# Optimization experiments

Measured on AMD Instinct MI355X. Metric: run time of the kernel, lower is better.

Reference implementation:

```python
import jax, jax.numpy as jnp
import numpy as np

NUM_HEADS = 8


def _forward(x, Wq, bq, Wk, bk, Wv, bv, Wo, bo, w1, b1, w2, b2, tau):
    B, S, E = x.shape
    H = NUM_HEADS
    hd = E // H
    scale = hd ** -0.5

    def heads(t):
        return t.reshape(B, S, H, hd).transpose(0, 2, 1, 3)  # [B,H,S,hd]

    q = heads(x @ Wq + bq)
    k = heads(x @ Wk + bk)
    v = heads(x @ Wv + bv)
    s = jnp.einsum('bhqd,bhkd->bhqk', q, k) * scale  # [B,H,S,S]

    # ---- autopoietic transform (vectorized over batch, no mask) ----
    s = jnp.clip(jnp.nan_to_num(s, nan=0.0, posinf=10.0, neginf=-10.0), -15.0, 15.0)
    ma = s.mean(axis=1)  # mean over heads -> [B,S,S]
    eps_safe = 0.05  # clamp(eps=1e-6, 0.05, 0.8)
    sa = jnp.clip(jnp.clip(ma, -8.0, 8.0) * eps_safe, -10.0, 10.0)
    # 1x1 conv on [1,1,S,S] == per-channel scalar scale+bias -> [B,C,S,S]
    hid = jax.nn.relu(jnp.clip(sa[:, None] * w1[None, :, None, None]
                               + b1[None, :, None, None], -5.0, 5.0))
    ap = jnp.clip(jnp.einsum('bcij,c->bij', hid, w2) + b2, -5.0, 5.0)
    taylor = jnp.clip(1.0 + 0.05 * (ap * 50.0), 0.5, 1.5)
    sig = jax.nn.sigmoid(taylor)
    p = jax.nn.softmax(jnp.clip(ma, -10.0, 10.0), axis=-1)
    Hent = -p * jnp.log(p + 1e-6)
    Fm = jax.nn.softmax(3.0 * Hent, axis=-1)
    t = sig * Fm
    eo = jnp.sqrt((ma * ma).sum(axis=(1, 2), keepdims=True)) + 1e-4  # fro norm
    et = jnp.sqrt((t * t).sum(axis=(1, 2), keepdims=True)) + 1e-4
    t = jnp.clip(eo / et, 0.8, 1.2) * t
    tm = t.mean(axis=(1, 2), keepdims=True)
    om = ma.mean(axis=(1, 2), keepdims=True)
    tstd = jnp.sqrt(jnp.clip(((t - tm) ** 2).mean(axis=(1, 2), keepdims=True), 0.01, None))
    ostd = jnp.sqrt(jnp.clip(((ma - om) ** 2).mean(axis=(1, 2), keepdims=True), 0.01, None))
    gd = jnp.clip(ostd / tstd, 0.8, 1.2)
    ar = jnp.clip(jnp.abs(ma).max(axis=(1, 2), keepdims=True), 1.0, 10.0)
    sm = jnp.clip(0.3 / jnp.log1p(ar), 0.1, 0.5)
    st = tm + sm * gd * (t - tm)  # scaled_transform
    ent = Hent.mean(axis=(1, 2), keepdims=True)
    ne = ent / jnp.log(jnp.float32(S))  # normalized entropy (max_entropy = log S)
    rr = 0.4 * (1.0 - jnp.clip(ne, 0.0, 0.4))  # residual ratio (base 0.4, entropy-damped)
    # blend transform back into per-head scores (res_scale = 1.0)
    s = s + rr[:, None] * (st - ma)[:, None]

    attn = jax.nn.softmax(s / tau, axis=-1)
    out = jnp.einsum('bhqk,bhkd->bhqd', attn, v)
    out = out.transpose(0, 2, 1, 3).reshape(B, S, E)
    return out @ Wo + bo


def setup_inputs() -> dict:
    key = jax.random.key(0)
    ks = jax.random.split(key, 8)
    B, S, E, C = 4, 512, 512, 128
    w_scale = 0.02
    return {
        'x': jax.random.normal(ks[0], (B, S, E), dtype=jnp.float32),
        'Wq': jax.random.normal(ks[1], (E, E), dtype=jnp.float32) * w_scale,
        'bq': jnp.zeros((E,), jnp.float32),
        'Wk': jax.random.normal(ks[2], (E, E), dtype=jnp.float32) * w_scale,
        'bk': jnp.zeros((E,), jnp.float32),
        'Wv': jax.random.normal(ks[3], (E, E), dtype=jnp.float32) * w_scale,
        'bv': jnp.zeros((E,), jnp.float32),
        'Wo': jax.random.normal(ks[4], (E, E), dtype=jnp.float32) * w_scale,
        'bo': jnp.zeros((E,), jnp.float32),
        'w1': jax.random.normal(ks[5], (C,), dtype=jnp.float32) * 0.5,
        'b1': jnp.zeros((C,), jnp.float32),
        'w2': jax.random.normal(ks[6], (C,), dtype=jnp.float32) * 0.1,
        'b2': jnp.zeros((1,), jnp.float32),
        'tau': jnp.ones((1,), jnp.float32),
    }


def reference(x, Wq, bq, Wk, bk, Wv, bv, Wo, bo, w1, b1, w2, b2, tau):
    return _forward(x, Wq, bq, Wk, bk, Wv, bv, Wo, bo, w1, b1, w2, b2, tau)
```

## Files before the change

kernel.cpp:

```cpp
#include <hip/hip_runtime.h>
#include <math.h>

#define BB 4
#define SS 512
#define EE 512
#define NH 8
#define HD 64
#define NC 128
#define NTAB 4096

typedef _Float16 f16x8 __attribute__((ext_vector_type(8)));
typedef float f32x4 __attribute__((ext_vector_type(4)));

struct HL { _Float16 h, l; };

__device__ __forceinline__ float clampf(float v, float lo, float hi) {
  return fminf(fmaxf(v, lo), hi);
}
__device__ __forceinline__ HL split16(float x) {
  HL r;
  r.h = (_Float16)x;
  r.l = (_Float16)(x - (float)r.h);
  return r;
}

__device__ __forceinline__ float waveRedSum(float v) {
#pragma unroll
  for (int o = 32; o; o >>= 1) v += __shfl_xor(v, o);
  return v;
}
__device__ __forceinline__ float waveRedMax(float v) {
#pragma unroll
  for (int o = 32; o; o >>= 1) v = fmaxf(v, __shfl_xor(v, o));
  return v;
}
__device__ __forceinline__ float blockRedSum(float v, float* red) {
  int tid = threadIdx.x;
  v = waveRedSum(v);
  __syncthreads();
  if ((tid & 63) == 0) red[tid >> 6] = v;
  __syncthreads();
  return red[0] + red[1] + red[2] + red[3];
}
__device__ __forceinline__ float blockRedMax(float v, float* red) {
  int tid = threadIdx.x;
  v = waveRedMax(v);
  __syncthreads();
  if ((tid & 63) == 0) red[tid >> 6] = v;
  __syncthreads();
  return fmaxf(fmaxf(red[0], red[1]), fmaxf(red[2], red[3]));
}

__global__ __launch_bounds__(256) void k_prep(
    const float* __restrict__ Wq, const float* __restrict__ Wk,
    const float* __restrict__ Wv, const float* __restrict__ Wo,
    _Float16* __restrict__ Wth, _Float16* __restrict__ Wtl) {
  const int j = blockIdx.x;
  const int tid = threadIdx.x;
  const int z = j >> 6;
  const int rem = j & 63;
  const int k0 = (rem & 7) * 64, n0 = (rem >> 3) * 64;
  const float* W = (z == 0) ? Wq : (z == 1) ? Wk : (z == 2) ? Wv : Wo;
  __shared__ float Tt[64][68];
  const int r = tid >> 2, c = (tid & 3) * 16;
#pragma unroll
  for (int jj = 0; jj < 16; jj += 4)
    *(float4*)&Tt[r][c + jj] =
        *(const float4*)(W + (size_t)(k0 + r) * EE + n0 + c + jj);
  __syncthreads();
  f16x8 h0, l0, h1, l1;
#pragma unroll
  for (int jj = 0; jj < 8; ++jj) {
    HL r0 = split16(Tt[c + jj][r]);
    HL r1 = split16(Tt[c + 8 + jj][r]);
    h0[jj] = r0.h; l0[jj] = r0.l;
    h1[jj] = r1.h; l1[jj] = r1.l;
  }
  _Float16* dh = Wth + ((size_t)z * EE + n0 + r) * EE + k0 + c;
  _Float16* dl = Wtl + ((size_t)z * EE + n0 + r) * EE + k0 + c;
  *(f16x8*)dh = h0;
  *(f16x8*)(dh + 8) = h1;
  *(f16x8*)dl = l0;
  *(f16x8*)(dl + 8) = l1;
}

__global__ __launch_bounds__(256) void k_qkv_mfma(
    const float* __restrict__ x,
    const _Float16* __restrict__ Wth, const _Float16* __restrict__ Wtl,
    const float* __restrict__ bq, const float* __restrict__ bk,
    const float* __restrict__ bv, const float* __restrict__ w1,
    const float* __restrict__ b1, const float* __restrict__ w2,
    const float* __restrict__ b2, float* __restrict__ T,
    _Float16* __restrict__ qh, _Float16* __restrict__ ql,
    _Float16* __restrict__ kh, _Float16* __restrict__ kl,
    _Float16* __restrict__ vth, _Float16* __restrict__ vtl) {
  const int which = blockIdx.z;
  const int tid = threadIdx.x;
  const int wave = tid >> 6, lane = tid & 63;
  const int quad = lane >> 4, l16 = lane & 15;
  const int m0 = blockIdx.y * 64;
  const int n0 = blockIdx.x * 64;
  const _Float16* Bh = Wth + (size_t)which * EE * EE;
  const _Float16* Bl = Wtl + (size_t)which * EE * EE;

  __shared__ __align__(16) char smpool[36864];
  _Float16(*LAh)[72] = (_Float16(*)[72])(smpool);
  _Float16(*LAl)[72] = (_Float16(*)[72])(smpool + 9216);
  _Float16(*LBh)[72] = (_Float16(*)[72])(smpool + 18432);
  _Float16(*LBl)[72] = (_Float16(*)[72])(smpool + 27648);
  float(*TR)[68] = (float(*)[68])(smpool);

  const int sr0 = tid >> 3, sc0 = (tid & 7) * 8;
  const int sr1 = sr0 + 32;

  float4 rx0a = *(const float4*)(x + (size_t)(m0 + sr0) * EE + sc0);
  float4 rx0b = *(const float4*)(x + (size_t)(m0 + sr0) * EE + sc0 + 4);
  float4 rx1a = *(const float4*)(x + (size_t)(m0 + sr1) * EE + sc0);
  float4 rx1b = *(const float4*)(x + (size_t)(m0 + sr1) * EE + sc0 + 4);
  f16x8 rB0h = *(const f16x8*)(Bh + (size_t)(n0 + sr0) * EE + sc0);
  f16x8 rB0l = *(const f16x8*)(Bl + (size_t)(n0 + sr0) * EE + sc0);
  f16x8 rB1h = *(const f16x8*)(Bh + (size_t)(n0 + sr1) * EE + sc0);
  f16x8 rB1l = *(const f16x8*)(Bl + (size_t)(n0 + sr1) * EE + sc0);

  f32x4 acc[4] = {};
  for (int k0 = 0; k0 < EE; k0 += 64) {
    if (k0) __syncthreads();
    {
      float f0[8] = {rx0a.x, rx0a.y, rx0a.z, rx0a.w,
                     rx0b.x, rx0b.y, rx0b.z, rx0b.w};
      float f1[8] = {rx1a.x, rx1a.y, rx1a.z, rx1a.w,
                     rx1b.x, rx1b.y, rx1b.z, rx1b.w};
      f16x8 h0, l0, h1, l1;
#pragma unroll
      for (int j = 0; j < 8; ++j) {
        HL r0 = split16(f0[j]);
        HL r1 = split16(f1[j]);
        h0[j] = r0.h; l0[j] = r0.l;
        h1[j] = r1.h; l1[j] = r1.l;
      }
      *(f16x8*)&LAh[sr0][sc0] = h0;
      *(f16x8*)&LAl[sr0][sc0] = l0;
      *(f16x8*)&LAh[sr1][sc0] = h1;
      *(f16x8*)&LAl[sr1][sc0] = l1;
    }
    *(f16x8*)&LBh[sr0][sc0] = rB0h;
    *(f16x8*)&LBl[sr0][sc0] = rB0l;
    *(f16x8*)&LBh[sr1][sc0] = rB1h;
    *(f16x8*)&LBl[sr1][sc0] = rB1l;
    __syncthreads();
    if (k0 + 64 < EE) {
      const int kn = k0 + 64;
      rx0a = *(const float4*)(x + (size_t)(m0 + sr0) * EE + kn + sc0);
      rx0b = *(const float4*)(x + (size_t)(m0 + sr0) * EE + kn + sc0 + 4);
      rx1a = *(const float4*)(x + (size_t)(m0 + sr1) * EE + kn + sc0);
      rx1b = *(const float4*)(x + (size_t)(m0 + sr1) * EE + kn + sc0 + 4);
      rB0h = *(const f16x8*)(Bh + (size_t)(n0 + sr0) * EE + kn + sc0);
      rB0l = *(const f16x8*)(Bl + (size_t)(n0 + sr0) * EE + kn + sc0);
      rB1h = *(const f16x8*)(Bh + (size_t)(n0 + sr1) * EE + kn + sc0);
      rB1l = *(const f16x8*)(Bl + (size_t)(n0 + sr1) * EE + kn + sc0);
    }
#pragma unroll
    for (int kk = 0; kk < 64; kk += 32) {
      f16x8 ah = *(const f16x8*)&LAh[wave * 16 + l16][kk + quad * 8];
      f16x8 al = *(const f16x8*)&LAl[wave * 16 + l16][kk + quad * 8];
#pragma unroll
      for (int nt = 0; nt < 4; ++nt) {
        f16x8 bhf = *(const f16x8*)&LBh[nt * 16 + l16][kk + quad * 8];
        f16x8 blf = *(const f16x8*)&LBl[nt * 16 + l16][kk + quad * 8];
        acc[nt] = __builtin_amdgcn_mfma_f32_16x16x32_f16(ah, bhf, acc[nt], 0, 0, 0);
        acc[nt] = __builtin_amdgcn_mfma_f32_16x16x32_f16(ah, blf, acc[nt], 0, 0, 0);
        acc[nt] = __builtin_amdgcn_mfma_f32_16x16x32_f16(al, bhf, acc[nt], 0, 0, 0);
      }
    }
  }
  const float* bias = (which == 0) ? bq : (which == 1) ? bk : bv;
  if (which == 2) {
    __syncthreads();
#pragma unroll
    for (int nt = 0; nt < 4; ++nt) {
      const int dcol = nt * 16 + l16;
      const float bb = bias[n0 + nt * 16 + l16];
#pragma unroll
      for (int r = 0; r < 4; ++r)
        TR[dcol][wave * 16 + quad * 4 + r] = acc[nt][r] + bb;
    }
    __syncthreads();
    const int d = tid >> 2, cc = (tid & 3) * 16;
    const int bh = (m0 >> 9) * NH + (n0 >> 6);
    const int si0 = m0 & 511;
    f16x8 h0, l0, h1, l1;
#pragma unroll
    for (int jj = 0; jj < 8; ++jj) {
      HL r0 = split16(TR[d][cc + jj]);
      HL r1 = split16(TR[d][cc + 8 + jj]);
      h0[jj] = r0.h; l0[jj] = r0.l;
      h1[jj] = r1.h; l1[jj] = r1.l;
    }
    _Float16* dh = vth + ((size_t)bh * HD + d) * SS + si0 + cc;
    _Float16* dl = vtl + ((size_t)bh * HD + d) * SS + si0 + cc;
    *(f16x8*)dh = h0;
    *(f16x8*)(dh + 8) = h1;
    *(f16x8*)dl = l0;
    *(f16x8*)(dl + 8) = l1;
  } else {
    const float postscale = (which == 0) ? 0.125f : 1.0f;
    const int mbase = m0 + wave * 16 + quad * 4;
#pragma unroll
    for (int nt = 0; nt < 4; ++nt) {
      const int col = n0 + nt * 16 + l16;
      const float bb = bias[col];
      const int hh = col >> 6, d = col & 63;
#pragma unroll
      for (int r = 0; r < 4; ++r) {
        const int mm = mbase + r;
        const int b_ = mm >> 9, si = mm & 511;
        const size_t idx = (((size_t)(b_ * NH + hh)) * SS + si) * HD + d;
        const float val = (acc[nt][r] + bb) * postscale;
        HL sp = split16(val);
        (which ? kh : qh)[idx] = sp.h;
        (which ? kl : ql)[idx] = sp.l;
      }
    }
    if (which == 0 && blockIdx.x == 0 && blockIdx.y < 17) {
      int idx = blockIdx.y * 256 + tid;
      if (idx <= NTAB) {
        float sa = -0.4f + (float)idx * (0.8f / (float)NTAB);
        float ap = 0.f;
#pragma unroll 4
        for (int c = 0; c < NC; ++c) {
          float h = fminf(fmaxf(sa * w1[c] + b1[c], 0.f), 5.f);
          ap += h * w2[c];
        }
        ap = clampf(ap + b2[0], -5.f, 5.f);
        float tay = clampf(1.0f + 0.05f * (ap * 50.0f), 0.5f, 1.5f);
        T[idx] = 1.0f / (1.0f + expf(-tay));
      }
    }
  }
}

__global__ __launch_bounds__(256) void k_scores_mfma(
    const _Float16* __restrict__ qh, const _Float16* __restrict__ ql,
    const _Float16* __restrict__ kh, const _Float16* __restrict__ kl,
    float* __restrict__ s) {
  const int bh = blockIdx.z;
  const int i0 = blockIdx.y * 64, j0 = blockIdx.x * 64;
  const int tid = threadIdx.x;
  const int wave = tid >> 6, lane = tid & 63;
  const int quad = lane >> 4, l16 = lane & 15;

  __shared__ _Float16 Qh[64][72], Ql[64][72], Kh[64][72], Kl[64][72];
  const int r = tid >> 2, c = (tid & 3) * 16;
  {
    const size_t qoff = ((size_t)bh * SS + i0 + r) * HD + c;
    const size_t koff = ((size_t)bh * SS + j0 + r) * HD + c;
    *(f16x8*)&Qh[r][c] = *(const f16x8*)(qh + qoff);
    *(f16x8*)&Qh[r][c + 8] = *(const f16x8*)(qh + qoff + 8);
    *(f16x8*)&Ql[r][c] = *(const f16x8*)(ql + qoff);
    *(f16x8*)&Ql[r][c + 8] = *(const f16x8*)(ql + qoff + 8);
    *(f16x8*)&Kh[r][c] = *(const f16x8*)(kh + koff);
    *(f16x8*)&Kh[r][c + 8] = *(const f16x8*)(kh + koff + 8);
    *(f16x8*)&Kl[r][c] = *(const f16x8*)(kl + koff);
    *(f16x8*)&Kl[r][c + 8] = *(const f16x8*)(kl + koff + 8);
  }
  __syncthreads();

  f16x8 a_hi[2], a_lo[2];
#pragma unroll
  for (int ks = 0; ks < 2; ++ks) {
    a_hi[ks] = *(const f16x8*)&Qh[wave * 16 + l16][ks * 32 + quad * 8];
    a_lo[ks] = *(const f16x8*)&Ql[wave * 16 + l16][ks * 32 + quad * 8];
  }
  f32x4 acc[4] = {};
#pragma unroll
  for (int ks = 0; ks < 2; ++ks) {
#pragma unroll
    for (int t = 0; t < 4; ++t) {
      f16x8 b_hi = *(const f16x8*)&Kh[t * 16 + l16][ks * 32 + quad * 8];
      f16x8 b_lo = *(const f16x8*)&Kl[t * 16 + l16][ks * 32 + quad * 8];
      acc[t] = __builtin_amdgcn_mfma_f32_16x16x32_f16(a_hi[ks], b_hi,
                                                      acc[t], 0, 0, 0);
      acc[t] = __builtin_amdgcn_mfma_f32_16x16x32_f16(a_hi[ks], b_lo,
                                                      acc[t], 0, 0, 0);
      acc[t] = __builtin_amdgcn_mfma_f32_16x16x32_f16(a_lo[ks], b_hi,
                                                      acc[t], 0, 0, 0);
    }
  }
  float* sb = s + (size_t)bh * SS * SS;
#pragma unroll
  for (int t = 0; t < 4; ++t) {
#pragma unroll
    for (int r2 = 0; r2 < 4; ++r2) {
      float val = clampf(acc[t][r2], -15.0f, 15.0f);
      sb[(size_t)(i0 + wave * 16 + quad * 4 + r2) * SS + j0 + t * 16 + l16] = val;
    }
  }
}

__global__ __launch_bounds__(64) void k_rowstat(
    const float* __restrict__ s, const float* __restrict__ T,
    float* __restrict__ ma, float* __restrict__ t_un,
    float* __restrict__ rowred) {
  const int row = blockIdx.x;
  const int b_ = row >> 9, i = row & 511;
  const int lane = threadIdx.x;

  float4 a0 = {0.f, 0.f, 0.f, 0.f}, a1 = {0.f, 0.f, 0.f, 0.f};
#pragma unroll
  for (int hh = 0; hh < NH; ++hh) {
    const float4* p = reinterpret_cast<const float4*>(
                          s + (((size_t)(b_ * NH + hh) * SS) + i) * SS) +
                      lane * 2;
    float4 u0 = p[0], u1 = p[1];
    a0.x += u0.x; a0.y += u0.y; a0.z += u0.z; a0.w += u0.w;
    a1.x += u1.x; a1.y += u1.y; a1.z += u1.z; a1.w += u1.w;
  }
  float m[8] = {a0.x * 0.125f, a0.y * 0.125f, a0.z * 0.125f, a0.w * 0.125f,
                a1.x * 0.125f, a1.y * 0.125f, a1.z * 0.125f, a1.w * 0.125f};
  {
    float4* mp = reinterpret_cast<float4*>(ma + ((size_t)b_ * SS + i) * SS) +
                 lane * 2;
    float4 w0 = {m[0], m[1], m[2], m[3]}, w1v = {m[4], m[5], m[6], m[7]};
    mp[0] = w0;
    mp[1] = w1v;
  }
  float sma = 0.f, sma2 = 0.f, mabs = 0.f;
#pragma unroll
  for (int e = 0; e < 8; ++e) {
    sma += m[e];
    sma2 += m[e] * m[e];
    mabs = fmaxf(mabs, fabsf(m[e]));
  }
  sma = waveRedSum(sma);
  sma2 = waveRedSum(sma2);
  mabs = waveRedMax(mabs);

  float ex[8], esum = 0.f;
#pragma unroll
  for (int e = 0; e < 8; ++e) {
    ex[e] = expf(clampf(m[e], -10.f, 10.f));
    esum += ex[e];
  }
  esum = waveRedSum(esum);
  float inv = 1.0f / esum;
  float Hv[8], sH = 0.f;
#pragma unroll
  for (int e = 0; e < 8; ++e) {
    float p = ex[e] * inv;
    Hv[e] = -p * logf(p + 1e-6f);
    sH += Hv[e];
  }
  sH = waveRedSum(sH);

  float fx[8], fsum = 0.f;
#pragma unroll
  for (int e = 0; e < 8; ++e) {
    fx[e] = expf(3.0f * Hv[e]);
    fsum += fx[e];
  }
  fsum = waveRedSum(fsum);
  float finv = 1.0f / fsum;

  float t[8], st = 0.f, st2 = 0.f;
#pragma unroll
  for (int e = 0; e < 8; ++e) {
    float sa = clampf(m[e], -8.f, 8.f) * 0.05f;
    float pos = (sa + 0.4f) * ((float)NTAB / 0.8f);
    int idx = (int)pos;
    idx = idx < 0 ? 0 : (idx > NTAB - 1 ? NTAB - 1 : idx);
    float frac = pos - (float)idx;
    float g0 = T[idx], g1 = T[idx + 1];
    float sig = g0 + (g1 - g0) * frac;
    t[e] = sig * fx[e] * finv;
    st += t[e];
    st2 += t[e] * t[e];
  }
  st = waveRedSum(st);
  st2 = waveRedSum(st2);
  {
    float4* tp = reinterpret_cast<float4*>(t_un + ((size_t)b_ * SS + i) * SS) +
                 lane * 2;
    float4 w0 = {t[0], t[1], t[2], t[3]}, w1v = {t[4], t[5], t[6], t[7]};
    tp[0] = w0;
    tp[1] = w1v;
  }
  if (lane == 0) {
    float* rp = rowred + (size_t)row * 8;
    rp[0] = sma; rp[1] = sma2; rp[2] = mabs;
    rp[3] = st;  rp[4] = st2;  rp[5] = sH;
  }
}

__global__ __launch_bounds__(256) void k_av_fused(
    const float* __restrict__ s, const float* __restrict__ ma,
    const float* __restrict__ t_un, const float* __restrict__ rowred,
    const float* __restrict__ tau, const _Float16* __restrict__ vth,
    const _Float16* __restrict__ vtl, _Float16* __restrict__ oh,
    _Float16* __restrict__ ol) {
  const int bh = blockIdx.y;
  const int b_ = bh >> 3, hh = bh & 7;
  const int m0 = blockIdx.x * 32;
  const int tid = threadIdx.x;
  const int wave = tid >> 6, lane = tid & 63;
  const int quad = lane >> 4, l16 = lane & 15;

  __shared__ float red[4];
  float c0, c1, c2;
  {
    const float* r0 = rowred + ((size_t)b_ * SS + tid * 2) * 8;
    const float* r1 = r0 + 8;
    float sma = blockRedSum(r0[0] + r1[0], red);
    float sma2 = blockRedSum(r0[1] + r1[1], red);
    float mabs = blockRedMax(fmaxf(r0[2], r1[2]), red);
    float st = blockRedSum(r0[3] + r1[3], red);
    float st2 = blockRedSum(r0[4] + r1[4], red);
    float sH = blockRedSum(r0[5] + r1[5], red);
    const float N = (float)(SS * SS);
    float eo = sqrtf(sma2) + 1e-4f;
    float et = sqrtf(st2) + 1e-4f;
    float r = clampf(eo / et, 0.8f, 1.2f);
    float tmean = r * st / N;
    float om = sma / N;
    float vart = r * r * fmaxf(st2 / N - (st / N) * (st / N), 0.f);
    float tstd = sqrtf(fmaxf(vart, 0.01f));
    float varo = fmaxf(sma2 / N - om * om, 0.f);
    float ostd = sqrtf(fmaxf(varo, 0.01f));
    float gd = clampf(ostd / tstd, 0.8f, 1.2f);
    float ar = clampf(mabs, 1.f, 10.f);
    float sm = clampf(0.3f / log1pf(ar), 0.1f, 0.5f);
    float ent = sH / N;
    float ne = ent / logf((float)SS);
    float rr = 0.4f * (1.f - clampf(ne, 0.f, 0.4f));
    float G = sm * gd;
    c0 = rr * (1.f - G) * tmean;
    c1 = rr * G * r;
    c2 = rr;
  }
  const float itau = 1.0f / tau[0];

  __shared__ _Float16 Ph[32][40], Pl[32][40];
  __shared__ float Zp[32][4];

  const bool stager = (tid < 128);
  const int srow = tid >> 2;
  const int ci = tid & 3;
  const int schunk = ci * 8;
  const size_t sbase = ((size_t)bh * SS + m0 + (srow & 31)) * SS + schunk;
  const size_t mbase = ((size_t)b_ * SS + m0 + (srow & 31)) * SS + schunk;

  float4 sv0, sv1, mv0, mv1, tv0, tv1;
  if (stager) {
    sv0 = *(const float4*)(s + sbase);
    sv1 = *(const float4*)(s + sbase + 4);
    mv0 = *(const float4*)(ma + mbase);
    mv1 = *(const float4*)(ma + mbase + 4);
    tv0 = *(const float4*)(t_un + mbase);
    tv1 = *(const float4*)(t_un + mbase + 4);
  }

  float zpart = 0.f;
  f32x4 acc[2] = {};
  for (int k0 = 0; k0 < SS; k0 += 32) {
    if (k0) __syncthreads();
    if (stager) {
      float svv[8] = {sv0.x, sv0.y, sv0.z, sv0.w, sv1.x, sv1.y, sv1.z, sv1.w};
      float mvv[8] = {mv0.x, mv0.y, mv0.z, mv0.w, mv1.x, mv1.y, mv1.z, mv1.w};
      float tvv[8] = {tv0.x, tv0.y, tv0.z, tv0.w, tv1.x, tv1.y, tv1.z, tv1.w};
      f16x8 hv, lv;
#pragma unroll
      for (int j = 0; j < 8; ++j) {
        float vv = (svv[j] + c0 + c1 * tvv[j] - c2 * mvv[j]) * itau;
        float e = expf(vv) * 1.52587890625e-05f;
        zpart += e;
        HL r = split16(e);
        hv[j] = r.h;
        lv[j] = r.l;
      }
      *(f16x8*)&Ph[srow][schunk] = hv;
      *(f16x8*)&Pl[srow][schunk] = lv;
    }
    __syncthreads();
    if (stager && k0 + 32 < SS) {
      sv0 = *(const float4*)(s + sbase + k0 + 32);
      sv1 = *(const float4*)(s + sbase + k0 + 36);
      mv0 = *(const float4*)(ma + mbase + k0 + 32);
      mv1 = *(const float4*)(ma + mbase + k0 + 36);
      tv0 = *(const float4*)(t_un + mbase + k0 + 32);
      tv1 = *(const float4*)(t_un + mbase + k0 + 36);
    }
    const size_t boff = ((size_t)bh * HD + wave * 16 + l16) * SS + k0 + quad * 8;
    f16x8 bh_ = *(const f16x8*)(vth + boff);
    f16x8 bl_ = *(const f16x8*)(vtl + boff);
#pragma unroll
    for (int mt = 0; mt < 2; ++mt) {
      f16x8 ah = *(const f16x8*)&Ph[mt * 16 + l16][quad * 8];
      f16x8 al = *(const f16x8*)&Pl[mt * 16 + l16][quad * 8];
      acc[mt] = __builtin_amdgcn_mfma_f32_16x16x32_f16(ah, bh_, acc[mt], 0, 0, 0);
      acc[mt] = __builtin_amdgcn_mfma_f32_16x16x32_f16(ah, bl_, acc[mt], 0, 0, 0);
      acc[mt] = __builtin_amdgcn_mfma_f32_16x16x32_f16(al, bh_, acc[mt], 0, 0, 0);
    }
  }
  __syncthreads();
  if (stager) Zp[srow][ci] = zpart;
  __syncthreads();
#pragma unroll
  for (int mt = 0; mt < 2; ++mt) {
#pragma unroll
    for (int r = 0; r < 4; ++r) {
      const int lr = mt * 16 + quad * 4 + r;
      const float Z = Zp[lr][0] + Zp[lr][1] + Zp[lr][2] + Zp[lr][3];
      const float oV = acc[mt][r] / Z;
      const int si = m0 + lr;
      const size_t idx =
          ((size_t)(b_ * SS + si)) * EE + hh * HD + wave * 16 + l16;
      HL sp = split16(oV);
      oh[idx] = sp.h;
      ol[idx] = sp.l;
    }
  }
}

__global__ __launch_bounds__(256) void k_out_mfma(
    const _Float16* __restrict__ oh, const _Float16* __restrict__ ol,
    const _Float16* __restrict__ Wth, const _Float16* __restrict__ Wtl,
    const float* __restrict__ bo, float* __restrict__ out) {
  const int tid = threadIdx.x;
  const int wave = tid >> 6, lane = tid & 63;
  const int quad = lane >> 4, l16 = lane & 15;
  const int m0 = blockIdx.y * 64;
  const int n0 = blockIdx.x * 64;
  const _Float16* Bh = Wth + (size_t)3 * EE * EE;
  const _Float16* Bl = Wtl + (size_t)3 * EE * EE;

  __shared__ _Float16 LAh[64][72], LAl[64][72], LBh[64][72], LBl[64][72];

  const int sr0 = tid >> 3, sc0 = (tid & 7) * 8;
  const int sr1 = sr0 + 32;

  f16x8 rA0h = *(const f16x8*)(oh + (size_t)(m0 + sr0) * EE + sc0);
  f16x8 rA0l = *(const f16x8*)(ol + (size_t)(m0 + sr0) * EE + sc0);
  f16x8 rB0h = *(const f16x8*)(Bh + (size_t)(n0 + sr0) * EE + sc0);
  f16x8 rB0l = *(const f16x8*)(Bl + (size_t)(n0 + sr0) * EE + sc0);
  f16x8 rA1h = *(const f16x8*)(oh + (size_t)(m0 + sr1) * EE + sc0);
  f16x8 rA1l = *(const f16x8*)(ol + (size_t)(m0 + sr1) * EE + sc0);
  f16x8 rB1h = *(const f16x8*)(Bh + (size_t)(n0 + sr1) * EE + sc0);
  f16x8 rB1l = *(const f16x8*)(Bl + (size_t)(n0 + sr1) * EE + sc0);

  f32x4 acc[4] = {};
  for (int k0 = 0; k0 < EE; k0 += 64) {
    if (k0) __syncthreads();
    *(f16x8*)&LAh[sr0][sc0] = rA0h;
    *(f16x8*)&LAl[sr0][sc0] = rA0l;
    *(f16x8*)&LBh[sr0][sc0] = rB0h;
    *(f16x8*)&LBl[sr0][sc0] = rB0l;
    *(f16x8*)&LAh[sr1][sc0] = rA1h;
    *(f16x8*)&LAl[sr1][sc0] = rA1l;
    *(f16x8*)&LBh[sr1][sc0] = rB1h;
    *(f16x8*)&LBl[sr1][sc0] = rB1l;
    __syncthreads();
    if (k0 + 64 < EE) {
      const int kn = k0 + 64;
      rA0h = *(const f16x8*)(oh + (size_t)(m0 + sr0) * EE + kn + sc0);
      rA0l = *(const f16x8*)(ol + (size_t)(m0 + sr0) * EE + kn + sc0);
      rB0h = *(const f16x8*)(Bh + (size_t)(n0 + sr0) * EE + kn + sc0);
      rB0l = *(const f16x8*)(Bl + (size_t)(n0 + sr0) * EE + kn + sc0);
      rA1h = *(const f16x8*)(oh + (size_t)(m0 + sr1) * EE + kn + sc0);
      rA1l = *(const f16x8*)(ol + (size_t)(m0 + sr1) * EE + kn + sc0);
      rB1h = *(const f16x8*)(Bh + (size_t)(n0 + sr1) * EE + kn + sc0);
      rB1l = *(const f16x8*)(Bl + (size_t)(n0 + sr1) * EE + kn + sc0);
    }
#pragma unroll
    for (int kk = 0; kk < 64; kk += 32) {
      f16x8 ah = *(const f16x8*)&LAh[wave * 16 + l16][kk + quad * 8];
      f16x8 al = *(const f16x8*)&LAl[wave * 16 + l16][kk + quad * 8];
#pragma unroll
      for (int nt = 0; nt < 4; ++nt) {
        f16x8 bhf = *(const f16x8*)&LBh[nt * 16 + l16][kk + quad * 8];
        f16x8 blf = *(const f16x8*)&LBl[nt * 16 + l16][kk + quad * 8];
        acc[nt] = __builtin_amdgcn_mfma_f32_16x16x32_f16(ah, bhf, acc[nt], 0, 0, 0);
        acc[nt] = __builtin_amdgcn_mfma_f32_16x16x32_f16(ah, blf, acc[nt], 0, 0, 0);
        acc[nt] = __builtin_amdgcn_mfma_f32_16x16x32_f16(al, bhf, acc[nt], 0, 0, 0);
      }
    }
  }
  const int mbase = m0 + wave * 16 + quad * 4;
#pragma unroll
  for (int nt = 0; nt < 4; ++nt) {
    const int col = n0 + nt * 16 + l16;
    const float bb = bo[col];
#pragma unroll
    for (int r = 0; r < 4; ++r) {
      const int m = mbase + r;
      out[(size_t)m * EE + col] = acc[nt][r] + bb;
    }
  }
}

extern "C" void kernel_launch(void* const* d_in, const int* in_sizes, int n_in,
                              void* d_out, int out_size, void* d_ws,
                              size_t ws_size, hipStream_t stream) {
  const float* x = (const float*)d_in[0];
  const float* Wq = (const float*)d_in[1];
  const float* bq = (const float*)d_in[2];
  const float* Wk = (const float*)d_in[3];
  const float* bk = (const float*)d_in[4];
  const float* Wv = (const float*)d_in[5];
  const float* bv = (const float*)d_in[6];
  const float* Wo = (const float*)d_in[7];
  const float* bo = (const float*)d_in[8];
  const float* w1 = (const float*)d_in[9];
  const float* b1 = (const float*)d_in[10];
  const float* w2 = (const float*)d_in[11];
  const float* b2 = (const float*)d_in[12];
  const float* tau = (const float*)d_in[13];
  float* out = (float*)d_out;

  const size_t NX = (size_t)2048 * EE;
  const size_t NW = (size_t)4 * EE * EE;
  const size_t NQK = (size_t)BB * NH * SS * HD;
  const size_t NS = (size_t)BB * NH * SS * SS;

  _Float16* Wth = (_Float16*)d_ws;
  _Float16* Wtl = Wth + NW;
  _Float16* qh = Wtl + NW;
  _Float16* ql = qh + NQK;
  _Float16* kh = ql + NQK;
  _Float16* kl = kh + NQK;
  _Float16* vth = kl + NQK;
  _Float16* vtl = vth + NQK;
  _Float16* oh = vtl + NQK;
  _Float16* ol = oh + NX;
  float* s = (float*)(ol + NX);
  float* ma = s + NS;
  float* t_un = ma + (size_t)BB * SS * SS;
  float* T = t_un + (size_t)BB * SS * SS;
  float* rowred = T + 8192;

  k_prep<<<256, 256, 0, stream>>>(Wq, Wk, Wv, Wo, Wth, Wtl);
  k_qkv_mfma<<<dim3(8, 32, 3), 256, 0, stream>>>(x, Wth, Wtl, bq, bk, bv, w1,
                                                 b1, w2, b2, T, qh, ql, kh, kl,
                                                 vth, vtl);
  k_scores_mfma<<<dim3(8, 8, 32), 256, 0, stream>>>(qh, ql, kh, kl, s);
  k_rowstat<<<2048, 64, 0, stream>>>(s, T, ma, t_un, rowred);
  k_av_fused<<<dim3(16, 32), 256, 0, stream>>>(s, ma, t_un, rowred, tau, vth,
                                               vtl, oh, ol);
  k_out_mfma<<<dim3(8, 32), 256, 0, stream>>>(oh, ol, Wth, Wtl, bo, out);
}
```

Before: 160.3 us.

## Fuse all stages into one cooperative persistent kernel with grid syncs

Replaces the six separate kernel launches (weight prep, QKV GEMM, scores, row stats, AV, output projection) with a single cooperative kernel of 512 blocks that loops over work items per stage and uses grid.sync between stages. The intent is to remove per-launch overhead and the gaps between launches. In exchange, each stage now runs on a fixed 512-block grid with grid-wide barriers. Stages that previously used more blocks now loop with less latency hiding, and occupancy is bounded by the cooperative launch limit.

```diff
diff --git a/kernel.cpp b/kernel.cpp
--- a/kernel.cpp
+++ b/kernel.cpp
@@ -1,5 +1,8 @@
 #include <hip/hip_runtime.h>
+#include <hip/hip_cooperative_groups.h>
 #include <math.h>
+
+namespace cg = cooperative_groups;
 
 #define BB 4
 #define SS 512
@@ -34,7 +37,7 @@
   for (int o = 32; o; o >>= 1) v = fmaxf(v, __shfl_xor(v, o));
   return v;
 }
-__device__ __forceinline__ float blockRedSum(float v, float* red) {
+__device__ __forceinline__ float blockRedSum(float v, volatile float* red) {
   int tid = threadIdx.x;
   v = waveRedSum(v);
   __syncthreads();
@@ -42,7 +45,7 @@
   __syncthreads();
   return red[0] + red[1] + red[2] + red[3];
 }
-__device__ __forceinline__ float blockRedMax(float v, float* red) {
+__device__ __forceinline__ float blockRedMax(float v, volatile float* red) {
   int tid = threadIdx.x;
   v = waveRedMax(v);
   __syncthreads();
@@ -51,547 +54,539 @@
   return fmaxf(fmaxf(red[0], red[1]), fmaxf(red[2], red[3]));
 }
 
-__global__ __launch_bounds__(256) void k_prep(
-    const float* __restrict__ Wq, const float* __restrict__ Wk,
-    const float* __restrict__ Wv, const float* __restrict__ Wo,
-    _Float16* __restrict__ Wth, _Float16* __restrict__ Wtl) {
-  const int j = blockIdx.x;
-  const int tid = threadIdx.x;
-  const int z = j >> 6;
-  const int rem = j & 63;
-  const int k0 = (rem & 7) * 64, n0 = (rem >> 3) * 64;
-  const float* W = (z == 0) ? Wq : (z == 1) ? Wk : (z == 2) ? Wv : Wo;
-  __shared__ float Tt[64][68];
-  const int r = tid >> 2, c = (tid & 3) * 16;
-#pragma unroll
-  for (int jj = 0; jj < 16; jj += 4)
-    *(float4*)&Tt[r][c + jj] =
-        *(const float4*)(W + (size_t)(k0 + r) * EE + n0 + c + jj);
-  __syncthreads();
-  f16x8 h0, l0, h1, l1;
-#pragma unroll
-  for (int jj = 0; jj < 8; ++jj) {
-    HL r0 = split16(Tt[c + jj][r]);
-    HL r1 = split16(Tt[c + 8 + jj][r]);
-    h0[jj] = r0.h; l0[jj] = r0.l;
-    h1[jj] = r1.h; l1[jj] = r1.l;
-  }
-  _Float16* dh = Wth + ((size_t)z * EE + n0 + r) * EE + k0 + c;
-  _Float16* dl = Wtl + ((size_t)z * EE + n0 + r) * EE + k0 + c;
-  *(f16x8*)dh = h0;
-  *(f16x8*)(dh + 8) = h1;
-  *(f16x8*)dl = l0;
-  *(f16x8*)(dl + 8) = l1;
-}
-
-__global__ __launch_bounds__(256) void k_qkv_mfma(
-    const float* __restrict__ x,
-    const _Float16* __restrict__ Wth, const _Float16* __restrict__ Wtl,
-    const float* __restrict__ bq, const float* __restrict__ bk,
-    const float* __restrict__ bv, const float* __restrict__ w1,
-    const float* __restrict__ b1, const float* __restrict__ w2,
-    const float* __restrict__ b2, float* __restrict__ T,
-    _Float16* __restrict__ qh, _Float16* __restrict__ ql,
-    _Float16* __restrict__ kh, _Float16* __restrict__ kl,
-    _Float16* __restrict__ vth, _Float16* __restrict__ vtl) {
-  const int which = blockIdx.z;
+struct Params {
+  const float *x, *Wq, *bq, *Wk, *bk, *Wv, *bv, *Wo, *bo;
+  const float *w1, *b1, *w2, *b2, *tau;
+  float* out;
+  _Float16 *Wth, *Wtl, *qh, *ql, *kh, *kl, *vth, *vtl, *oh, *ol;
+  float *s, *ma, *t_un, *T, *rowred;
+};
+
+__global__ __launch_bounds__(256) void k_fused(Params p) {
+  cg::grid_group grid = cg::this_grid();
+  const int bid = blockIdx.x;
   const int tid = threadIdx.x;
   const int wave = tid >> 6, lane = tid & 63;
   const int quad = lane >> 4, l16 = lane & 15;
-  const int m0 = blockIdx.y * 64;
-  const int n0 = blockIdx.x * 64;
-  const _Float16* Bh = Wth + (size_t)which * EE * EE;
-  const _Float16* Bl = Wtl + (size_t)which * EE * EE;
-
-  __shared__ __align__(16) char smpool[36864];
-  _Float16(*LAh)[72] = (_Float16(*)[72])(smpool);
-  _Float16(*LAl)[72] = (_Float16(*)[72])(smpool + 9216);
-  _Float16(*LBh)[72] = (_Float16(*)[72])(smpool + 18432);
-  _Float16(*LBl)[72] = (_Float16(*)[72])(smpool + 27648);
-  float(*TR)[68] = (float(*)[68])(smpool);
-
-  const int sr0 = tid >> 3, sc0 = (tid & 7) * 8;
-  const int sr1 = sr0 + 32;
-
-  float4 rx0a = *(const float4*)(x + (size_t)(m0 + sr0) * EE + sc0);
-  float4 rx0b = *(const float4*)(x + (size_t)(m0 + sr0) * EE + sc0 + 4);
-  float4 rx1a = *(const float4*)(x + (size_t)(m0 + sr1) * EE + sc0);
-  float4 rx1b = *(const float4*)(x + (size_t)(m0 + sr1) * EE + sc0 + 4);
-  f16x8 rB0h = *(const f16x8*)(Bh + (size_t)(n0 + sr0) * EE + sc0);
-  f16x8 rB0l = *(const f16x8*)(Bl + (size_t)(n0 + sr0) * EE + sc0);
-  f16x8 rB1h = *(const f16x8*)(Bh + (size_t)(n0 + sr1) * EE + sc0);
-  f16x8 rB1l = *(const f16x8*)(Bl + (size_t)(n0 + sr1) * EE + sc0);
-
-  f32x4 acc[4] = {};
-  for (int k0 = 0; k0 < EE; k0 += 64) {
-    if (k0) __syncthreads();
-    {
-      float f0[8] = {rx0a.x, rx0a.y, rx0a.z, rx0a.w,
-                     rx0b.x, rx0b.y, rx0b.z, rx0b.w};
-      float f1[8] = {rx1a.x, rx1a.y, rx1a.z, rx1a.w,
-                     rx1b.x, rx1b.y, rx1b.z, rx1b.w};
-      f16x8 h0, l0, h1, l1;
-#pragma unroll
-      for (int j = 0; j < 8; ++j) {
-        HL r0 = split16(f0[j]);
-        HL r1 = split16(f1[j]);
-        h0[j] = r0.h; l0[j] = r0.l;
-        h1[j] = r1.h; l1[j] = r1.l;
-      }
-      *(f16x8*)&LAh[sr0][sc0] = h0;
-      *(f16x8*)&LAl[sr0][sc0] = l0;
-      *(f16x8*)&LAh[sr1][sc0] = h1;
-      *(f16x8*)&LAl[sr1][sc0] = l1;
-    }
-    *(f16x8*)&LBh[sr0][sc0] = rB0h;
-    *(f16x8*)&LBl[sr0][sc0] = rB0l;
-    *(f16x8*)&LBh[sr1][sc0] = rB1h;
-    *(f16x8*)&LBl[sr1][sc0] = rB1l;
+
+  __shared__ __align__(16) char pool[36864];
+  __shared__ float redS[4];
+
+  if (bid < 256) {
+    const int z = bid >> 6;
+    const int rem = bid & 63;
+    const int k0 = (rem & 7) * 64, n0 = (rem >> 3) * 64;
+    const float* W = (z == 0) ? p.Wq : (z == 1) ? p.Wk : (z == 2) ? p.Wv : p.Wo;
+    float(*Tt)[68] = (float(*)[68])pool;
+    const int r = tid >> 2, c = (tid & 3) * 16;
+#pragma unroll
+    for (int jj = 0; jj < 16; jj += 4)
+      *(float4*)&Tt[r][c + jj] =
+          *(const float4*)(W + (size_t)(k0 + r) * EE + n0 + c + jj);
     __syncthreads();
-    if (k0 + 64 < EE) {
-      const int kn = k0 + 64;
-      rx0a = *(const float4*)(x + (size_t)(m0 + sr0) * EE + kn + sc0);
-      rx0b = *(const float4*)(x + (size_t)(m0 + sr0) * EE + kn + sc0 + 4);
-      rx1a = *(const float4*)(x + (size_t)(m0 + sr1) * EE + kn + sc0);
-      rx1b = *(const float4*)(x + (size_t)(m0 + sr1) * EE + kn + sc0 + 4);
-      rB0h = *(const f16x8*)(Bh + (size_t)(n0 + sr0) * EE + kn + sc0);
-      rB0l = *(const f16x8*)(Bl + (size_t)(n0 + sr0) * EE + kn + sc0);
-      rB1h = *(const f16x8*)(Bh + (size_t)(n0 + sr1) * EE + kn + sc0);
-      rB1l = *(const f16x8*)(Bl + (size_t)(n0 + sr1) * EE + kn + sc0);
-    }
-#pragma unroll
-    for (int kk = 0; kk < 64; kk += 32) {
-      f16x8 ah = *(const f16x8*)&LAh[wave * 16 + l16][kk + quad * 8];
-      f16x8 al = *(const f16x8*)&LAl[wave * 16 + l16][kk + quad * 8];
-#pragma unroll
-      for (int nt = 0; nt < 4; ++nt) {
-        f16x8 bhf = *(const f16x8*)&LBh[nt * 16 + l16][kk + quad * 8];
-        f16x8 blf = *(const f16x8*)&LBl[nt * 16 + l16][kk + quad * 8];
-        acc[nt] = __builtin_amdgcn_mfma_f32_16x16x32_f16(ah, bhf, acc[nt], 0, 0, 0);
-        acc[nt] = __builtin_amdgcn_mfma_f32_16x16x32_f16(ah, blf, acc[nt], 0, 0, 0);
-        acc[nt] = __builtin_amdgcn_mfma_f32_16x16x32_f16(al, bhf, acc[nt], 0, 0, 0);
-      }
-    }
-  }
-  const float* bias = (which == 0) ? bq : (which == 1) ? bk : bv;
-  if (which == 2) {
-    __syncthreads();
-#pragma unroll
-    for (int nt = 0; nt < 4; ++nt) {
-      const int dcol = nt * 16 + l16;
-      const float bb = bias[n0 + nt * 16 + l16];
-#pragma unroll
-      for (int r = 0; r < 4; ++r)
-        TR[dcol][wave * 16 + quad * 4 + r] = acc[nt][r] + bb;
-    }
-    __syncthreads();
-    const int d = tid >> 2, cc = (tid & 3) * 16;
-    const int bh = (m0 >> 9) * NH + (n0 >> 6);
-    const int si0 = m0 & 511;
     f16x8 h0, l0, h1, l1;
 #pragma unroll
     for (int jj = 0; jj < 8; ++jj) {
-      HL r0 = split16(TR[d][cc + jj]);
-      HL r1 = split16(TR[d][cc + 8 + jj]);
+      HL r0 = split16(Tt[c + jj][r]);
+      HL r1 = split16(Tt[c + 8 + jj][r]);
       h0[jj] = r0.h; l0[jj] = r0.l;
       h1[jj] = r1.h; l1[jj] = r1.l;
     }
-    _Float16* dh = vth + ((size_t)bh * HD + d) * SS + si0 + cc;
-    _Float16* dl = vtl + ((size_t)bh * HD + d) * SS + si0 + cc;
+    _Float16* dh = p.Wth + ((size_t)z * EE + n0 + r) * EE + k0 + c;
+    _Float16* dl = p.Wtl + ((size_t)z * EE + n0 + r) * EE + k0 + c;
     *(f16x8*)dh = h0;
     *(f16x8*)(dh + 8) = h1;
     *(f16x8*)dl = l0;
     *(f16x8*)(dl + 8) = l1;
-  } else {
-    const float postscale = (which == 0) ? 0.125f : 1.0f;
+  } else if (bid < 273) {
+    int idx = (bid - 256) * 256 + tid;
+    if (idx <= NTAB) {
+      float sa = -0.4f + (float)idx * (0.8f / (float)NTAB);
+      float ap = 0.f;
+#pragma unroll 4
+      for (int c = 0; c < NC; ++c) {
+        float h = fminf(fmaxf(sa * p.w1[c] + p.b1[c], 0.f), 5.f);
+        ap += h * p.w2[c];
+      }
+      ap = clampf(ap + p.b2[0], -5.f, 5.f);
+      float tay = clampf(1.0f + 0.05f * (ap * 50.0f), 0.5f, 1.5f);
+      p.T[idx] = 1.0f / (1.0f + expf(-tay));
+    }
+  }
+  grid.sync();
+
+  {
+    _Float16(*LAh)[72] = (_Float16(*)[72])(pool);
+    _Float16(*LAl)[72] = (_Float16(*)[72])(pool + 9216);
+    _Float16(*LBh)[72] = (_Float16(*)[72])(pool + 18432);
+    _Float16(*LBl)[72] = (_Float16(*)[72])(pool + 27648);
+    float(*TR)[68] = (float(*)[68])(pool);
+    const int sr0 = tid >> 3, sc0 = (tid & 7) * 8;
+    const int sr1 = sr0 + 32;
+    for (int item = bid; item < 768; item += 512) {
+      __syncthreads();
+      const int which = item >> 8;
+      const int rem = item & 255;
+      const int m0 = (rem >> 3) * 64;
+      const int n0 = (rem & 7) * 64;
+      const _Float16* Bh = p.Wth + (size_t)which * EE * EE;
+      const _Float16* Bl = p.Wtl + (size_t)which * EE * EE;
+
+      float4 rx0a = *(const float4*)(p.x + (size_t)(m0 + sr0) * EE + sc0);
+      float4 rx0b = *(const float4*)(p.x + (size_t)(m0 + sr0) * EE + sc0 + 4);
+      float4 rx1a = *(const float4*)(p.x + (size_t)(m0 + sr1) * EE + sc0);
+      float4 rx1b = *(const float4*)(p.x + (size_t)(m0 + sr1) * EE + sc0 + 4);
+      f16x8 rB0h = *(const f16x8*)(Bh + (size_t)(n0 + sr0) * EE + sc0);
+      f16x8 rB0l = *(const f16x8*)(Bl + (size_t)(n0 + sr0) * EE + sc0);
+      f16x8 rB1h = *(const f16x8*)(Bh + (size_t)(n0 + sr1) * EE + sc0);
+      f16x8 rB1l = *(const f16x8*)(Bl + (size_t)(n0 + sr1) * EE + sc0);
+
+      f32x4 acc[4] = {};
+      for (int k0 = 0; k0 < EE; k0 += 64) {
+        if (k0) __syncthreads();
+        {
+          float f0[8] = {rx0a.x, rx0a.y, rx0a.z, rx0a.w,
+                         rx0b.x, rx0b.y, rx0b.z, rx0b.w};
+          float f1[8] = {rx1a.x, rx1a.y, rx1a.z, rx1a.w,
+                         rx1b.x, rx1b.y, rx1b.z, rx1b.w};
+          f16x8 h0, l0, h1, l1;
+#pragma unroll
+          for (int j = 0; j < 8; ++j) {
+            HL r0 = split16(f0[j]);
+            HL r1 = split16(f1[j]);
+            h0[j] = r0.h; l0[j] = r0.l;
+            h1[j] = r1.h; l1[j] = r1.l;
+          }
+          *(f16x8*)&LAh[sr0][sc0] = h0;
+          *(f16x8*)&LAl[sr0][sc0] = l0;
+          *(f16x8*)&LAh[sr1][sc0] = h1;
+          *(f16x8*)&LAl[sr1][sc0] = l1;
+        }
+        *(f16x8*)&LBh[sr0][sc0] = rB0h;
+        *(f16x8*)&LBl[sr0][sc0] = rB0l;
+        *(f16x8*)&LBh[sr1][sc0] = rB1h;
+        *(f16x8*)&LBl[sr1][sc0] = rB1l;
+        __syncthreads();
+        if (k0 + 64 < EE) {
+          const int kn = k0 + 64;
+          rx0a = *(const float4*)(p.x + (size_t)(m0 + sr0) * EE + kn + sc0);
+          rx0b = *(const float4*)(p.x + (size_t)(m0 + sr0) * EE + kn + sc0 + 4);
+          rx1a = *(const float4*)(p.x + (size_t)(m0 + sr1) * EE + kn + sc0);
+          rx1b = *(const float4*)(p.x + (size_t)(m0 + sr1) * EE + kn + sc0 + 4);
+          rB0h = *(const f16x8*)(Bh + (size_t)(n0 + sr0) * EE + kn + sc0);
+          rB0l = *(const f16x8*)(Bl + (size_t)(n0 + sr0) * EE + kn + sc0);
+          rB1h = *(const f16x8*)(Bh + (size_t)(n0 + sr1) * EE + kn + sc0);
+          rB1l = *(const f16x8*)(Bl + (size_t)(n0 + sr1) * EE + kn + sc0);
+        }
+#pragma unroll
+        for (int kk = 0; kk < 64; kk += 32) {
+          f16x8 ah = *(const f16x8*)&LAh[wave * 16 + l16][kk + quad * 8];
+          f16x8 al = *(const f16x8*)&LAl[wave * 16 + l16][kk + quad * 8];
+#pragma unroll
+          for (int nt = 0; nt < 4; ++nt) {
+            f16x8 bhf = *(const f16x8*)&LBh[nt * 16 + l16][kk + quad * 8];
+            f16x8 blf = *(const f16x8*)&LBl[nt * 16 + l16][kk + quad * 8];
+            acc[nt] = __builtin_amdgcn_mfma_f32_16x16x32_f16(ah, bhf, acc[nt], 0, 0, 0);
+            acc[nt] = __builtin_amdgcn_mfma_f32_16x16x32_f16(ah, blf, acc[nt], 0, 0, 0);
+            acc[nt] = __builtin_amdgcn_mfma_f32_16x16x32_f16(al, bhf, acc[nt], 0, 0, 0);
+          }
+        }
+      }
+      const float* bias = (which == 0) ? p.bq : (which == 1) ? p.bk : p.bv;
+      if (which == 2) {
+        __syncthreads();
+#pragma unroll
+        for (int nt = 0; nt < 4; ++nt) {
+          const int dcol = nt * 16 + l16;
+          const float bb = bias[n0 + nt * 16 + l16];
+#pragma unroll
+          for (int r = 0; r < 4; ++r)
+            TR[dcol][wave * 16 + quad * 4 + r] = acc[nt][r] + bb;
+        }
+        __syncthreads();
+        const int d = tid >> 2, cc = (tid & 3) * 16;
+        const int bh = (m0 >> 9) * NH + (n0 >> 6);
+        const int si0 = m0 & 511;
+        f16x8 h0, l0, h1, l1;
+#pragma unroll
+        for (int jj = 0; jj < 8; ++jj) {
+          HL r0 = split16(TR[d][cc + jj]);
+          HL r1 = split16(TR[d][cc + 8 + jj]);
+          h0[jj] = r0.h; l0[jj] = r0.l;
+          h1[jj] = r1.h; l1[jj] = r1.l;
+        }
+        _Float16* dh = p.vth + ((size_t)bh * HD + d) * SS + si0 + cc;
+        _Float16* dl = p.vtl + ((size_t)bh * HD + d) * SS + si0 + cc;
+        *(f16x8*)dh = h0;
+        *(f16x8*)(dh + 8) = h1;
+        *(f16x8*)dl = l0;
+        *(f16x8*)(dl + 8) = l1;
+      } else {
+        const float postscale = (which == 0) ? 0.125f : 1.0f;
+        const int mbase = m0 + wave * 16 + quad * 4;
+#pragma unroll
+        for (int nt = 0; nt < 4; ++nt) {
+          const int col = n0 + nt * 16 + l16;
+          const float bb = bias[col];
+          const int hh = col >> 6, d = col & 63;
+#pragma unroll
+          for (int r = 0; r < 4; ++r) {
+            const int mm = mbase + r;
+            const int b_ = mm >> 9, si = mm & 511;
+            const size_t idx = (((size_t)(b_ * NH + hh)) * SS + si) * HD + d;
+            const float val = (acc[nt][r] + bb) * postscale;
+            HL sp = split16(val);
+            (which ? p.kh : p.qh)[idx] = sp.h;
+            (which ? p.kl : p.ql)[idx] = sp.l;
+          }
+        }
+      }
+    }
+  }
+  grid.sync();
+
+  {
+    _Float16(*Qh)[72] = (_Float16(*)[72])(pool);
+    _Float16(*Ql)[72] = (_Float16(*)[72])(pool + 9216);
+    _Float16(*Kh)[72] = (_Float16(*)[72])(pool + 18432);
+    _Float16(*Kl)[72] = (_Float16(*)[72])(pool + 27648);
+    const int r = tid >> 2, c = (tid & 3) * 16;
+    for (int item = bid; item < 2048; item += 512) {
+      __syncthreads();
+      const int bh = item >> 6;
+      const int rem = item & 63;
+      const int i0 = (rem >> 3) * 64, j0 = (rem & 7) * 64;
+      {
+        const size_t qoff = ((size_t)bh * SS + i0 + r) * HD + c;
+        const size_t koff = ((size_t)bh * SS + j0 + r) * HD + c;
+        *(f16x8*)&Qh[r][c] = *(const f16x8*)(p.qh + qoff);
+        *(f16x8*)&Qh[r][c + 8] = *(const f16x8*)(p.qh + qoff + 8);
+        *(f16x8*)&Ql[r][c] = *(const f16x8*)(p.ql + qoff);
+        *(f16x8*)&Ql[r][c + 8] = *(const f16x8*)(p.ql + qoff + 8);
+        *(f16x8*)&Kh[r][c] = *(const f16x8*)(p.kh + koff);
+        *(f16x8*)&Kh[r][c + 8] = *(const f16x8*)(p.kh + koff + 8);
+        *(f16x8*)&Kl[r][c] = *(const f16x8*)(p.kl + koff);
+        *(f16x8*)&Kl[r][c + 8] = *(const f16x8*)(p.kl + koff + 8);
+      }
+      __syncthreads();
+      f16x8 a_hi[2], a_lo[2];
+#pragma unroll
+      for (int ks = 0; ks < 2; ++ks) {
+        a_hi[ks] = *(const f16x8*)&Qh[wave * 16 + l16][ks * 32 + quad * 8];
+        a_lo[ks] = *(const f16x8*)&Ql[wave * 16 + l16][ks * 32 + quad * 8];
+      }
+      f32x4 acc[4] = {};
+#pragma unroll
+      for (int ks = 0; ks < 2; ++ks) {
+#pragma unroll
+        for (int t = 0; t < 4; ++t) {
+          f16x8 b_hi = *(const f16x8*)&Kh[t * 16 + l16][ks * 32 + quad * 8];
+          f16x8 b_lo = *(const f16x8*)&Kl[t * 16 + l16][ks * 32 + quad * 8];
+          acc[t] = __builtin_amdgcn_mfma_f32_16x16x32_f16(a_hi[ks], b_hi,
+                                                          acc[t], 0, 0, 0);
+          acc[t] = __builtin_amdgcn_mfma_f32_16x16x32_f16(a_hi[ks], b_lo,
+                                                          acc[t], 0, 0, 0);
+          acc[t] = __builtin_amdgcn_mfma_f32_16x16x32_f16(a_lo[ks], b_hi,
+                                                          acc[t], 0, 0, 0);
+        }
+      }
+      float* sb = p.s + (size_t)bh * SS * SS;
+#pragma unroll
+      for (int t = 0; t < 4; ++t) {
+#pragma unroll
+        for (int r2 = 0; r2 < 4; ++r2) {
+          float val = clampf(acc[t][r2], -15.0f, 15.0f);
+          sb[(size_t)(i0 + wave * 16 + quad * 4 + r2) * SS + j0 + t * 16 + l16] =
+              val;
+        }
+      }
+    }
+  }
+  grid.sync();
+
+  {
+    const int row = bid * 4 + wave;
+    const int b_ = row >> 9, i = row & 511;
+    float4 a0 = {0.f, 0.f, 0.f, 0.f}, a1 = {0.f, 0.f, 0.f, 0.f};
+#pragma unroll
+    for (int hh = 0; hh < NH; ++hh) {
+      const float4* pr = reinterpret_cast<const float4*>(
+                             p.s + (((size_t)(b_ * NH + hh) * SS) + i) * SS) +
+                         lane * 2;
+      float4 u0 = pr[0], u1 = pr[1];
+      a0.x += u0.x; a0.y += u0.y; a0.z += u0.z; a0.w += u0.w;
+      a1.x += u1.x; a1.y += u1.y; a1.z += u1.z; a1.w += u1.w;
+    }
+    float m[8] = {a0.x * 0.125f, a0.y * 0.125f, a0.z * 0.125f, a0.w * 0.125f,
+                  a1.x * 0.125f, a1.y * 0.125f, a1.z * 0.125f, a1.w * 0.125f};
+    {
+      float4* mp = reinterpret_cast<float4*>(p.ma + ((size_t)b_ * SS + i) * SS) +
+                   lane * 2;
+      float4 w0 = {m[0], m[1], m[2], m[3]}, w1v = {m[4], m[5], m[6], m[7]};
+      mp[0] = w0;
+      mp[1] = w1v;
+    }
+    float sma = 0.f, sma2 = 0.f, mabs = 0.f;
+#pragma unroll
+    for (int e = 0; e < 8; ++e) {
+      sma += m[e];
+      sma2 += m[e] * m[e];
+      mabs = fmaxf(mabs, fabsf(m[e]));
+    }
+    sma = waveRedSum(sma);
+    sma2 = waveRedSum(sma2);
+    mabs = waveRedMax(mabs);
+
+    float ex[8], esum = 0.f;
+#pragma unroll
+    for (int e = 0; e < 8; ++e) {
+      ex[e] = expf(clampf(m[e], -10.f, 10.f));
+      esum += ex[e];
+    }
+    esum = waveRedSum(esum);
+    float inv = 1.0f / esum;
+    float Hv[8], sH = 0.f;
+#pragma unroll
+    for (int e = 0; e < 8; ++e) {
+      float pp = ex[e] * inv;
+      Hv[e] = -pp * logf(pp + 1e-6f);
+      sH += Hv[e];
+    }
+    sH = waveRedSum(sH);
+
+    float fx[8], fsum = 0.f;
+#pragma unroll
+    for (int e = 0; e < 8; ++e) {
+      fx[e] = expf(3.0f * Hv[e]);
+      fsum += fx[e];
+    }
+    fsum = waveRedSum(fsum);
+    float finv = 1.0f / fsum;
+
+    float t[8], st = 0.f, st2 = 0.f;
+#pragma unroll
+    for (int e = 0; e < 8; ++e) {
+      float sa = clampf(m[e], -8.f, 8.f) * 0.05f;
+      float pos = (sa + 0.4f) * ((float)NTAB / 0.8f);
+      int idx = (int)pos;
+      idx = idx < 0 ? 0 : (idx > NTAB - 1 ? NTAB - 1 : idx);
+      float frac = pos - (float)idx;
+      float g0 = p.T[idx], g1 = p.T[idx + 1];
+      float sig = g0 + (g1 - g0) * frac;
+      t[e] = sig * fx[e] * finv;
+      st += t[e];
+      st2 += t[e] * t[e];
+    }
+    st = waveRedSum(st);
+    st2 = waveRedSum(st2);
+    {
+      float4* tp =
+          reinterpret_cast<float4*>(p.t_un + ((size_t)b_ * SS + i) * SS) +
+          lane * 2;
+      float4 w0 = {t[0], t[1], t[2], t[3]}, w1v = {t[4], t[5], t[6], t[7]};
+      tp[0] = w0;
+      tp[1] = w1v;
+    }
+    if (lane == 0) {
+      float* rp = p.rowred + (size_t)row * 8;
+      rp[0] = sma; rp[1] = sma2; rp[2] = mabs;
+      rp[3] = st;  rp[4] = st2;  rp[5] = sH;
+    }
+  }
+  grid.sync();
+
+  {
+    const int item = bid;
+    const int bh = item >> 4;
+    const int b_ = bh >> 3, hh = bh & 7;
+    const int m0 = (item & 15) * 32;
+
+    float c0, c1, c2;
+    {
+      const float* r0 = p.rowred + ((size_t)b_ * SS + tid * 2) * 8;
+      const float* r1 = r0 + 8;
+      float sma = blockRedSum(r0[0] + r1[0], redS);
+      float sma2 = blockRedSum(r0[1] + r1[1], redS);
+      float mabs = blockRedMax(fmaxf(r0[2], r1[2]), redS);
+      float st = blockRedSum(r0[3] + r1[3], redS);
+      float st2 = blockRedSum(r0[4] + r1[4], redS);
+      float sH = blockRedSum(r0[5] + r1[5], redS);
+      const float N = (float)(SS * SS);
+      float eo = sqrtf(sma2) + 1e-4f;
+      float et = sqrtf(st2) + 1e-4f;
+      float r = clampf(eo / et, 0.8f, 1.2f);
+      float tmean = r * st / N;
+      float om = sma / N;
+      float vart = r * r * fmaxf(st2 / N - (st / N) * (st / N), 0.f);
+      float tstd = sqrtf(fmaxf(vart, 0.01f));
+      float varo = fmaxf(sma2 / N - om * om, 0.f);
+      float ostd = sqrtf(fmaxf(varo, 0.01f));
+      float gd = clampf(ostd / tstd, 0.8f, 1.2f);
+      float ar = clampf(mabs, 1.f, 10.f);
+      float sm = clampf(0.3f / log1pf(ar), 0.1f, 0.5f);
+      float ent = sH / N;
+      float ne = ent / logf((float)SS);
+      float rr = 0.4f * (1.f - clampf(ne, 0.f, 0.4f));
+      float G = sm * gd;
+      c0 = rr * (1.f - G) * tmean;
+      c1 = rr * G * r;
+      c2 = rr;
+    }
+    const float itau = 1.0f / p.tau[0];
+
+    _Float16(*Ph)[40] = (_Float16(*)[40])(pool);
+    _Float16(*Pl)[40] = (_Float16(*)[40])(pool + 2560);
+    float(*Zp)[4] = (float(*)[4])(pool + 5120);
+
+    const bool stager = (tid < 128);
+    const int srow = tid >> 2;
+    const int ci = tid & 3;
+    const int schunk = ci * 8;
+    const size_t sbase = ((size_t)bh * SS + m0 + (srow & 31)) * SS + schunk;
+    const size_t mbase = ((size_t)b_ * SS + m0 + (srow & 31)) * SS + schunk;
+
+    float4 sv0, sv1, mv0, mv1, tv0, tv1;
+    if (stager) {
+      sv0 = *(const float4*)(p.s + sbase);
+      sv1 = *(const float4*)(p.s + sbase + 4);
+      mv0 = *(const float4*)(p.ma + mbase);
+      mv1 = *(const float4*)(p.ma + mbase + 4);
+      tv0 = *(const float4*)(p.t_un + mbase);
+      tv1 = *(const float4*)(p.t_un + mbase + 4);
+    }
+
+    float zpart = 0.f;
+    f32x4 acc[2] = {};
+    for (int k0 = 0; k0 < SS; k0 += 32) {
+      __syncthreads();
+      if (stager) {
+        float svv[8] = {sv0.x, sv0.y, sv0.z, sv0.w, sv1.x, sv1.y, sv1.z, sv1.w};
+        float mvv[8] = {mv0.x, mv0.y, mv0.z, mv0.w, mv1.x, mv1.y, mv1.z, mv1.w};
+        float tvv[8] = {tv0.x, tv0.y, tv0.z, tv0.w, tv1.x, tv1.y, tv1.z, tv1.w};
+        f16x8 hv, lv;
+#pragma unroll
+        for (int j = 0; j < 8; ++j) {
+          float vv = (svv[j] + c0 + c1 * tvv[j] - c2 * mvv[j]) * itau;
+          float e = expf(vv) * 1.52587890625e-05f;
+          zpart += e;
+          HL r = split16(e);
+          hv[j] = r.h;
+          lv[j] = r.l;
+        }
+        *(f16x8*)&Ph[srow][schunk] = hv;
+        *(f16x8*)&Pl[srow][schunk] = lv;
+      }
+      __syncthreads();
+      if (stager && k0 + 32 < SS) {
+        sv0 = *(const float4*)(p.s + sbase + k0 + 32);
+        sv1 = *(const float4*)(p.s + sbase + k0 + 36);
+        mv0 = *(const float4*)(p.ma + mbase + k0 + 32);
+        mv1 = *(const float4*)(p.ma + mbase + k0 + 36);
+        tv0 = *(const float4*)(p.t_un + mbase + k0 + 32);
+        tv1 = *(const float4*)(p.t_un + mbase + k0 + 36);
+      }
+      const size_t boff =
+          ((size_t)bh * HD + wave * 16 + l16) * SS + k0 + quad * 8;
+      f16x8 bh_ = *(const f16x8*)(p.vth + boff);
+      f16x8 bl_ = *(const f16x8*)(p.vtl + boff);
+#pragma unroll
+      for (int mt = 0; mt < 2; ++mt) {
+        f16x8 ah = *(const f16x8*)&Ph[mt * 16 + l16][quad * 8];
+        f16x8 al = *(const f16x8*)&Pl[mt * 16 + l16][quad * 8];
+        acc[mt] = __builtin_amdgcn_mfma_f32_16x16x32_f16(ah, bh_, acc[mt], 0, 0, 0);
+        acc[mt] = __builtin_amdgcn_mfma_f32_16x16x32_f16(ah, bl_, acc[mt], 0, 0, 0);
+        acc[mt] = __builtin_amdgcn_mfma_f32_16x16x32_f16(al, bh_, acc[mt], 0, 0, 0);
+      }
+    }
+    __syncthreads();
+    if (stager) Zp[srow][ci] = zpart;
+    __syncthreads();
+#pragma unroll
+    for (int mt = 0; mt < 2; ++mt) {
+#pragma unroll
+      for (int r = 0; r < 4; ++r) {
+        const int lr = mt * 16 + quad * 4 + r;
+        const float Z = Zp[lr][0] + Zp[lr][1] + Zp[lr][2] + Zp[lr][3];
+        const float oV = acc[mt][r] / Z;
+        const int si = m0 + lr;
+        const size_t idx =
+            ((size_t)(b_ * SS + si)) * EE + hh * HD + wave * 16 + l16;
+        HL sp = split16(oV);
+        p.oh[idx] = sp.h;
+        p.ol[idx] = sp.l;
+      }
+    }
+  }
+  grid.sync();
+
+  if (bid < 256) {
+    const int m0 = (bid >> 3) * 64;
+    const int n0 = (bid & 7) * 64;
+    const _Float16* Bh = p.Wth + (size_t)3 * EE * EE;
+    const _Float16* Bl = p.Wtl + (size_t)3 * EE * EE;
+    _Float16(*LAh)[72] = (_Float16(*)[72])(pool);
+    _Float16(*LAl)[72] = (_Float16(*)[72])(pool + 9216);
+    _Float16(*LBh)[72] = (_Float16(*)[72])(pool + 18432);
+    _Float16(*LBl)[72] = (_Float16(*)[72])(pool + 27648);
+    const int sr0 = tid >> 3, sc0 = (tid & 7) * 8;
+    const int sr1 = sr0 + 32;
+
+    f16x8 rA0h = *(const f16x8*)(p.oh + (size_t)(m0 + sr0) * EE + sc0);
+    f16x8 rA0l = *(const f16x8*)(p.ol + (size_t)(m0 + sr0) * EE + sc0);
+    f16x8 rB0h = *(const f16x8*)(Bh + (size_t)(n0 + sr0) * EE + sc0);
+    f16x8 rB0l = *(const f16x8*)(Bl + (size_t)(n0 + sr0) * EE + sc0);
+    f16x8 rA1h = *(const f16x8*)(p.oh + (size_t)(m0 + sr1) * EE + sc0);
+    f16x8 rA1l = *(const f16x8*)(p.ol + (size_t)(m0 + sr1) * EE + sc0);
+    f16x8 rB1h = *(const f16x8*)(Bh + (size_t)(n0 + sr1) * EE + sc0);
+    f16x8 rB1l = *(const f16x8*)(Bl + (size_t)(n0 + sr1) * EE + sc0);
+
+    f32x4 acc[4] = {};
+    for (int k0 = 0; k0 < EE; k0 += 64) {
+      __syncthreads();
+      *(f16x8*)&LAh[sr0][sc0] = rA0h;
+      *(f16x8*)&LAl[sr0][sc0] = rA0l;
+      *(f16x8*)&LBh[sr0][sc0] = rB0h;
+      *(f16x8*)&LBl[sr0][sc0] = rB0l;
+      *(f16x8*)&LAh[sr1][sc0] = rA1h;
+      *(f16x8*)&LAl[sr1][sc0] = rA1l;
+      *(f16x8*)&LBh[sr1][sc0] = rB1h;
+      *(f16x8*)&LBl[sr1][sc0] = rB1l;
+      __syncthreads();
+      if (k0 + 64 < EE) {
+        const int kn = k0 + 64;
+        rA0h = *(const f16x8*)(p.oh + (size_t)(m0 + sr0) * EE + kn + sc0);
+        rA0l = *(const f16x8*)(p.ol + (size_t)(m0 + sr0) * EE + kn + sc0);
+        rB0h = *(const f16x8*)(Bh + (size_t)(n0 + sr0) * EE + kn + sc0);
+        rB0l = *(const f16x8*)(Bl + (size_t)(n0 + sr0) * EE + kn + sc0);
+        rA1h = *(const f16x8*)(p.oh + (size_t)(m0 + sr1) * EE + kn + sc0);
+        rA1l = *(const f16x8*)(p.ol + (size_t)(m0 + sr1) * EE + kn + sc0);
+        rB1h = *(const f16x8*)(Bh + (size_t)(n0 + sr1) * EE + kn + sc0);
+        rB1l = *(const f16x8*)(Bl + (size_t)(n0 + sr1) * EE + kn + sc0);
+      }
+#pragma unroll
+      for (int kk = 0; kk < 64; kk += 32) {
+        f16x8 ah = *(const f16x8*)&LAh[wave * 16 + l16][kk + quad * 8];
+        f16x8 al = *(const f16x8*)&LAl[wave * 16 + l16][kk + quad * 8];
+#pragma unroll
+        for (int nt = 0; nt < 4; ++nt) {
+          f16x8 bhf = *(const f16x8*)&LBh[nt * 16 + l16][kk + quad * 8];
+          f16x8 blf = *(const f16x8*)&LBl[nt * 16 + l16][kk + quad * 8];
+          acc[nt] = __builtin_amdgcn_mfma_f32_16x16x32_f16(ah, bhf, acc[nt], 0, 0, 0);
+          acc[nt] = __builtin_amdgcn_mfma_f32_16x16x32_f16(ah, blf, acc[nt], 0, 0, 0);
+          acc[nt] = __builtin_amdgcn_mfma_f32_16x16x32_f16(al, bhf, acc[nt], 0, 0, 0);
+        }
+      }
+    }
     const int mbase = m0 + wave * 16 + quad * 4;
 #pragma unroll
     for (int nt = 0; nt < 4; ++nt) {
       const int col = n0 + nt * 16 + l16;
-      const float bb = bias[col];
-      const int hh = col >> 6, d = col & 63;
+      const float bb = p.bo[col];
 #pragma unroll
       for (int r = 0; r < 4; ++r) {
-        const int mm = mbase + r;
-        const int b_ = mm >> 9, si = mm & 511;
-        const size_t idx = (((size_t)(b_ * NH + hh)) * SS + si) * HD + d;
-        const float val = (acc[nt][r] + bb) * postscale;
-        HL sp = split16(val);
-        (which ? kh : qh)[idx] = sp.h;
-        (which ? kl : ql)[idx] = sp.l;
-      }
-    }
-    if (which == 0 && blockIdx.x == 0 && blockIdx.y < 17) {
-      int idx = blockIdx.y * 256 + tid;
-      if (idx <= NTAB) {
-        float sa = -0.4f + (float)idx * (0.8f / (float)NTAB);
-        float ap = 0.f;
-#pragma unroll 4
-        for (int c = 0; c < NC; ++c) {
-          float h = fminf(fmaxf(sa * w1[c] + b1[c], 0.f), 5.f);
-          ap += h * w2[c];
-        }
-        ap = clampf(ap + b2[0], -5.f, 5.f);
-        float tay = clampf(1.0f + 0.05f * (ap * 50.0f), 0.5f, 1.5f);
-        T[idx] = 1.0f / (1.0f + expf(-tay));
-      }
-    }
-  }
-}
-
-__global__ __launch_bounds__(256) void k_scores_mfma(
-    const _Float16* __restrict__ qh, const _Float16* __restrict__ ql,
-    const _Float16* __restrict__ kh, const _Float16* __restrict__ kl,
-    float* __restrict__ s) {
-  const int bh = blockIdx.z;
-  const int i0 = blockIdx.y * 64, j0 = blockIdx.x * 64;
-  const int tid = threadIdx.x;
-  const int wave = tid >> 6, lane = tid & 63;
-  const int quad = lane >> 4, l16 = lane & 15;
-
-  __shared__ _Float16 Qh[64][72], Ql[64][72], Kh[64][72], Kl[64][72];
-  const int r = tid >> 2, c = (tid & 3) * 16;
-  {
-    const size_t qoff = ((size_t)bh * SS + i0 + r) * HD + c;
-    const size_t koff = ((size_t)bh * SS + j0 + r) * HD + c;
-    *(f16x8*)&Qh[r][c] = *(const f16x8*)(qh + qoff);
-    *(f16x8*)&Qh[r][c + 8] = *(const f16x8*)(qh + qoff + 8);
-    *(f16x8*)&Ql[r][c] = *(const f16x8*)(ql + qoff);
-    *(f16x8*)&Ql[r][c + 8] = *(const f16x8*)(ql + qoff + 8);
-    *(f16x8*)&Kh[r][c] = *(const f16x8*)(kh + koff);
-    *(f16x8*)&Kh[r][c + 8] = *(const f16x8*)(kh + koff + 8);
-    *(f16x8*)&Kl[r][c] = *(const f16x8*)(kl + koff);
-    *(f16x8*)&Kl[r][c + 8] = *(const f16x8*)(kl + koff + 8);
-  }
-  __syncthreads();
-
-  f16x8 a_hi[2], a_lo[2];
-#pragma unroll
-  for (int ks = 0; ks < 2; ++ks) {
-    a_hi[ks] = *(const f16x8*)&Qh[wave * 16 + l16][ks * 32 + quad * 8];
-    a_lo[ks] = *(const f16x8*)&Ql[wave * 16 + l16][ks * 32 + quad * 8];
-  }
-  f32x4 acc[4] = {};
-#pragma unroll
-  for (int ks = 0; ks < 2; ++ks) {
-#pragma unroll
-    for (int t = 0; t < 4; ++t) {
-      f16x8 b_hi = *(const f16x8*)&Kh[t * 16 + l16][ks * 32 + quad * 8];
-      f16x8 b_lo = *(const f16x8*)&Kl[t * 16 + l16][ks * 32 + quad * 8];
-      acc[t] = __builtin_amdgcn_mfma_f32_16x16x32_f16(a_hi[ks], b_hi,
-                                                      acc[t], 0, 0, 0);
-      acc[t] = __builtin_amdgcn_mfma_f32_16x16x32_f16(a_hi[ks], b_lo,
-                                                      acc[t], 0, 0, 0);
-      acc[t] = __builtin_amdgcn_mfma_f32_16x16x32_f16(a_lo[ks], b_hi,
-                                                      acc[t], 0, 0, 0);
-    }
-  }
-  float* sb = s + (size_t)bh * SS * SS;
-#pragma unroll
-  for (int t = 0; t < 4; ++t) {
-#pragma unroll
-    for (int r2 = 0; r2 < 4; ++r2) {
-      float val = clampf(acc[t][r2], -15.0f, 15.0f);
-      sb[(size_t)(i0 + wave * 16 + quad * 4 + r2) * SS + j0 + t * 16 + l16] = val;
-    }
-  }
-}
-
-__global__ __launch_bounds__(64) void k_rowstat(
-    const float* __restrict__ s, const float* __restrict__ T,
-    float* __restrict__ ma, float* __restrict__ t_un,
-    float* __restrict__ rowred) {
-  const int row = blockIdx.x;
-  const int b_ = row >> 9, i = row & 511;
-  const int lane = threadIdx.x;
-
-  float4 a0 = {0.f, 0.f, 0.f, 0.f}, a1 = {0.f, 0.f, 0.f, 0.f};
-#pragma unroll
-  for (int hh = 0; hh < NH; ++hh) {
-    const float4* p = reinterpret_cast<const float4*>(
-                          s + (((size_t)(b_ * NH + hh) * SS) + i) * SS) +
-                      lane * 2;
-    float4 u0 = p[0], u1 = p[1];
-    a0.x += u0.x; a0.y += u0.y; a0.z += u0.z; a0.w += u0.w;
-    a1.x += u1.x; a1.y += u1.y; a1.z += u1.z; a1.w += u1.w;
-  }
-  float m[8] = {a0.x * 0.125f, a0.y * 0.125f, a0.z * 0.125f, a0.w * 0.125f,
-                a1.x * 0.125f, a1.y * 0.125f, a1.z * 0.125f, a1.w * 0.125f};
-  {
-    float4* mp = reinterpret_cast<float4*>(ma + ((size_t)b_ * SS + i) * SS) +
-                 lane * 2;
-    float4 w0 = {m[0], m[1], m[2], m[3]}, w1v = {m[4], m[5], m[6], m[7]};
-    mp[0] = w0;
-    mp[1] = w1v;
-  }
-  float sma = 0.f, sma2 = 0.f, mabs = 0.f;
-#pragma unroll
-  for (int e = 0; e < 8; ++e) {
-    sma += m[e];
-    sma2 += m[e] * m[e];
-    mabs = fmaxf(mabs, fabsf(m[e]));
-  }
-  sma = waveRedSum(sma);
-  sma2 = waveRedSum(sma2);
-  mabs = waveRedMax(mabs);
-
-  float ex[8], esum = 0.f;
-#pragma unroll
-  for (int e = 0; e < 8; ++e) {
-    ex[e] = expf(clampf(m[e], -10.f, 10.f));
-    esum += ex[e];
-  }
-  esum = waveRedSum(esum);
-  float inv = 1.0f / esum;
-  float Hv[8], sH = 0.f;
-#pragma unroll
-  for (int e = 0; e < 8; ++e) {
-    float p = ex[e] * inv;
-    Hv[e] = -p * logf(p + 1e-6f);
-    sH += Hv[e];
-  }
-  sH = waveRedSum(sH);
-
-  float fx[8], fsum = 0.f;
-#pragma unroll
-  for (int e = 0; e < 8; ++e) {
-    fx[e] = expf(3.0f * Hv[e]);
-    fsum += fx[e];
-  }
-  fsum = waveRedSum(fsum);
-  float finv = 1.0f / fsum;
-
-  float t[8], st = 0.f, st2 = 0.f;
-#pragma unroll
-  for (int e = 0; e < 8; ++e) {
-    float sa = clampf(m[e], -8.f, 8.f) * 0.05f;
-    float pos = (sa + 0.4f) * ((float)NTAB / 0.8f);
-    int idx = (int)pos;
-    idx = idx < 0 ? 0 : (idx > NTAB - 1 ? NTAB - 1 : idx);
-    float frac = pos - (float)idx;
-    float g0 = T[idx], g1 = T[idx + 1];
-    float sig = g0 + (g1 - g0) * frac;
-    t[e] = sig * fx[e] * finv;
-    st += t[e];
-    st2 += t[e] * t[e];
-  }
-  st = waveRedSum(st);
-  st2 = waveRedSum(st2);
-  {
-    float4* tp = reinterpret_cast<float4*>(t_un + ((size_t)b_ * SS + i) * SS) +
-                 lane * 2;
-    float4 w0 = {t[0], t[1], t[2], t[3]}, w1v = {t[4], t[5], t[6], t[7]};
-    tp[0] = w0;
-    tp[1] = w1v;
-  }
-  if (lane == 0) {
-    float* rp = rowred + (size_t)row * 8;
-    rp[0] = sma; rp[1] = sma2; rp[2] = mabs;
-    rp[3] = st;  rp[4] = st2;  rp[5] = sH;
-  }
-}
-
-__global__ __launch_bounds__(256) void k_av_fused(
-    const float* __restrict__ s, const float* __restrict__ ma,
-    const float* __restrict__ t_un, const float* __restrict__ rowred,
-    const float* __restrict__ tau, const _Float16* __restrict__ vth,
-    const _Float16* __restrict__ vtl, _Float16* __restrict__ oh,
-    _Float16* __restrict__ ol) {
-  const int bh = blockIdx.y;
-  const int b_ = bh >> 3, hh = bh & 7;
-  const int m0 = blockIdx.x * 32;
-  const int tid = threadIdx.x;
-  const int wave = tid >> 6, lane = tid & 63;
-  const int quad = lane >> 4, l16 = lane & 15;
-
-  __shared__ float red[4];
-  float c0, c1, c2;
-  {
-    const float* r0 = rowred + ((size_t)b_ * SS + tid * 2) * 8;
-    const float* r1 = r0 + 8;
-    float sma = blockRedSum(r0[0] + r1[0], red);
-    float sma2 = blockRedSum(r0[1] + r1[1], red);
-    float mabs = blockRedMax(fmaxf(r0[2], r1[2]), red);
-    float st = blockRedSum(r0[3] + r1[3], red);
-    float st2 = blockRedSum(r0[4] + r1[4], red);
-    float sH = blockRedSum(r0[5] + r1[5], red);
-    const float N = (float)(SS * SS);
-    float eo = sqrtf(sma2) + 1e-4f;
-    float et = sqrtf(st2) + 1e-4f;
-    float r = clampf(eo / et, 0.8f, 1.2f);
-    float tmean = r * st / N;
-    float om = sma / N;
-    float vart = r * r * fmaxf(st2 / N - (st / N) * (st / N), 0.f);
-    float tstd = sqrtf(fmaxf(vart, 0.01f));
-    float varo = fmaxf(sma2 / N - om * om, 0.f);
-    float ostd = sqrtf(fmaxf(varo, 0.01f));
-    float gd = clampf(ostd / tstd, 0.8f, 1.2f);
-    float ar = clampf(mabs, 1.f, 10.f);
-    float sm = clampf(0.3f / log1pf(ar), 0.1f, 0.5f);
-    float ent = sH / N;
-    float ne = ent / logf((float)SS);
-    float rr = 0.4f * (1.f - clampf(ne, 0.f, 0.4f));
-    float G = sm * gd;
-    c0 = rr * (1.f - G) * tmean;
-    c1 = rr * G * r;
-    c2 = rr;
-  }
-  const float itau = 1.0f / tau[0];
-
-  __shared__ _Float16 Ph[32][40], Pl[32][40];
-  __shared__ float Zp[32][4];
-
-  const bool stager = (tid < 128);
-  const int srow = tid >> 2;
-  const int ci = tid & 3;
-  const int schunk = ci * 8;
-  const size_t sbase = ((size_t)bh * SS + m0 + (srow & 31)) * SS + schunk;
-  const size_t mbase = ((size_t)b_ * SS + m0 + (srow & 31)) * SS + schunk;
-
-  float4 sv0, sv1, mv0, mv1, tv0, tv1;
-  if (stager) {
-    sv0 = *(const float4*)(s + sbase);
-    sv1 = *(const float4*)(s + sbase + 4);
-    mv0 = *(const float4*)(ma + mbase);
-    mv1 = *(const float4*)(ma + mbase + 4);
-    tv0 = *(const float4*)(t_un + mbase);
-    tv1 = *(const float4*)(t_un + mbase + 4);
-  }
-
-  float zpart = 0.f;
-  f32x4 acc[2] = {};
-  for (int k0 = 0; k0 < SS; k0 += 32) {
-    if (k0) __syncthreads();
-    if (stager) {
-      float svv[8] = {sv0.x, sv0.y, sv0.z, sv0.w, sv1.x, sv1.y, sv1.z, sv1.w};
-      float mvv[8] = {mv0.x, mv0.y, mv0.z, mv0.w, mv1.x, mv1.y, mv1.z, mv1.w};
-      float tvv[8] = {tv0.x, tv0.y, tv0.z, tv0.w, tv1.x, tv1.y, tv1.z, tv1.w};
-      f16x8 hv, lv;
-#pragma unroll
-      for (int j = 0; j < 8; ++j) {
-        float vv = (svv[j] + c0 + c1 * tvv[j] - c2 * mvv[j]) * itau;
-        float e = expf(vv) * 1.52587890625e-05f;
-        zpart += e;
-        HL r = split16(e);
-        hv[j] = r.h;
-        lv[j] = r.l;
-      }
-      *(f16x8*)&Ph[srow][schunk] = hv;
-      *(f16x8*)&Pl[srow][schunk] = lv;
-    }
-    __syncthreads();
-    if (stager && k0 + 32 < SS) {
-      sv0 = *(const float4*)(s + sbase + k0 + 32);
-      sv1 = *(const float4*)(s + sbase + k0 + 36);
-      mv0 = *(const float4*)(ma + mbase + k0 + 32);
-      mv1 = *(const float4*)(ma + mbase + k0 + 36);
-      tv0 = *(const float4*)(t_un + mbase + k0 + 32);
-      tv1 = *(const float4*)(t_un + mbase + k0 + 36);
-    }
-    const size_t boff = ((size_t)bh * HD + wave * 16 + l16) * SS + k0 + quad * 8;
-    f16x8 bh_ = *(const f16x8*)(vth + boff);
-    f16x8 bl_ = *(const f16x8*)(vtl + boff);
-#pragma unroll
-    for (int mt = 0; mt < 2; ++mt) {
-      f16x8 ah = *(const f16x8*)&Ph[mt * 16 + l16][quad * 8];
-      f16x8 al = *(const f16x8*)&Pl[mt * 16 + l16][quad * 8];
-      acc[mt] = __builtin_amdgcn_mfma_f32_16x16x32_f16(ah, bh_, acc[mt], 0, 0, 0);
-      acc[mt] = __builtin_amdgcn_mfma_f32_16x16x32_f16(ah, bl_, acc[mt], 0, 0, 0);
-      acc[mt] = __builtin_amdgcn_mfma_f32_16x16x32_f16(al, bh_, acc[mt], 0, 0, 0);
-    }
-  }
-  __syncthreads();
-  if (stager) Zp[srow][ci] = zpart;
-  __syncthreads();
-#pragma unroll
-  for (int mt = 0; mt < 2; ++mt) {
-#pragma unroll
-    for (int r = 0; r < 4; ++r) {
-      const int lr = mt * 16 + quad * 4 + r;
-      const float Z = Zp[lr][0] + Zp[lr][1] + Zp[lr][2] + Zp[lr][3];
-      const float oV = acc[mt][r] / Z;
-      const int si = m0 + lr;
-      const size_t idx =
-          ((size_t)(b_ * SS + si)) * EE + hh * HD + wave * 16 + l16;
-      HL sp = split16(oV);
-      oh[idx] = sp.h;
-      ol[idx] = sp.l;
-    }
-  }
-}
-
-__global__ __launch_bounds__(256) void k_out_mfma(
-    const _Float16* __restrict__ oh, const _Float16* __restrict__ ol,
-    const _Float16* __restrict__ Wth, const _Float16* __restrict__ Wtl,
-    const float* __restrict__ bo, float* __restrict__ out) {
-  const int tid = threadIdx.x;
-  const int wave = tid >> 6, lane = tid & 63;
-  const int quad = lane >> 4, l16 = lane & 15;
-  const int m0 = blockIdx.y * 64;
-  const int n0 = blockIdx.x * 64;
-  const _Float16* Bh = Wth + (size_t)3 * EE * EE;
-  const _Float16* Bl = Wtl + (size_t)3 * EE * EE;
-
-  __shared__ _Float16 LAh[64][72], LAl[64][72], LBh[64][72], LBl[64][72];
-
-  const int sr0 = tid >> 3, sc0 = (tid & 7) * 8;
-  const int sr1 = sr0 + 32;
-
-  f16x8 rA0h = *(const f16x8*)(oh + (size_t)(m0 + sr0) * EE + sc0);
-  f16x8 rA0l = *(const f16x8*)(ol + (size_t)(m0 + sr0) * EE + sc0);
-  f16x8 rB0h = *(const f16x8*)(Bh + (size_t)(n0 + sr0) * EE + sc0);
-  f16x8 rB0l = *(const f16x8*)(Bl + (size_t)(n0 + sr0) * EE + sc0);
-  f16x8 rA1h = *(const f16x8*)(oh + (size_t)(m0 + sr1) * EE + sc0);
-  f16x8 rA1l = *(const f16x8*)(ol + (size_t)(m0 + sr1) * EE + sc0);
-  f16x8 rB1h = *(const f16x8*)(Bh + (size_t)(n0 + sr1) * EE + sc0);
-  f16x8 rB1l = *(const f16x8*)(Bl + (size_t)(n0 + sr1) * EE + sc0);
-
-  f32x4 acc[4] = {};
-  for (int k0 = 0; k0 < EE; k0 += 64) {
-    if (k0) __syncthreads();
-    *(f16x8*)&LAh[sr0][sc0] = rA0h;
-    *(f16x8*)&LAl[sr0][sc0] = rA0l;
-    *(f16x8*)&LBh[sr0][sc0] = rB0h;
-    *(f16x8*)&LBl[sr0][sc0] = rB0l;
-    *(f16x8*)&LAh[sr1][sc0] = rA1h;
-    *(f16x8*)&LAl[sr1][sc0] = rA1l;
-    *(f16x8*)&LBh[sr1][sc0] = rB1h;
-    *(f16x8*)&LBl[sr1][sc0] = rB1l;
-    __syncthreads();
-    if (k0 + 64 < EE) {
-      const int kn = k0 + 64;
-      rA0h = *(const f16x8*)(oh + (size_t)(m0 + sr0) * EE + kn + sc0);
-      rA0l = *(const f16x8*)(ol + (size_t)(m0 + sr0) * EE + kn + sc0);
-      rB0h = *(const f16x8*)(Bh + (size_t)(n0 + sr0) * EE + kn + sc0);
-      rB0l = *(const f16x8*)(Bl + (size_t)(n0 + sr0) * EE + kn + sc0);
-      rA1h = *(const f16x8*)(oh + (size_t)(m0 + sr1) * EE + kn + sc0);
-      rA1l = *(const f16x8*)(ol + (size_t)(m0 + sr1) * EE + kn + sc0);
-      rB1h = *(const f16x8*)(Bh + (size_t)(n0 + sr1) * EE + kn + sc0);
-      rB1l = *(const f16x8*)(Bl + (size_t)(n0 + sr1) * EE + kn + sc0);
-    }
-#pragma unroll
-    for (int kk = 0; kk < 64; kk += 32) {
-      f16x8 ah = *(const f16x8*)&LAh[wave * 16 + l16][kk + quad * 8];
-      f16x8 al = *(const f16x8*)&LAl[wave * 16 + l16][kk + quad * 8];
-#pragma unroll
-      for (int nt = 0; nt < 4; ++nt) {
-        f16x8 bhf = *(const f16x8*)&LBh[nt * 16 + l16][kk + quad * 8];
-        f16x8 blf = *(const f16x8*)&LBl[nt * 16 + l16][kk + quad * 8];
-        acc[nt] = __builtin_amdgcn_mfma_f32_16x16x32_f16(ah, bhf, acc[nt], 0, 0, 0);
-        acc[nt] = __builtin_amdgcn_mfma_f32_16x16x32_f16(ah, blf, acc[nt], 0, 0, 0);
-        acc[nt] = __builtin_amdgcn_mfma_f32_16x16x32_f16(al, bhf, acc[nt], 0, 0, 0);
-      }
-    }
-  }
-  const int mbase = m0 + wave * 16 + quad * 4;
-#pragma unroll
-  for (int nt = 0; nt < 4; ++nt) {
-    const int col = n0 + nt * 16 + l16;
-    const float bb = bo[col];
-#pragma unroll
-    for (int r = 0; r < 4; ++r) {
-      const int m = mbase + r;
-      out[(size_t)m * EE + col] = acc[nt][r] + bb;
+        const int m = mbase + r;
+        p.out[(size_t)m * EE + col] = acc[nt][r] + bb;
+      }
     }
   }
 }
@@ -599,22 +594,6 @@
 extern "C" void kernel_launch(void* const* d_in, const int* in_sizes, int n_in,
                               void* d_out, int out_size, void* d_ws,
                               size_t ws_size, hipStream_t stream) {
-  const float* x = (const float*)d_in[0];
-  const float* Wq = (const float*)d_in[1];
-  const float* bq = (const float*)d_in[2];
-  const float* Wk = (const float*)d_in[3];
-  const float* bk = (const float*)d_in[4];
-  const float* Wv = (const float*)d_in[5];
-  const float* bv = (const float*)d_in[6];
-  const float* Wo = (const float*)d_in[7];
-  const float* bo = (const float*)d_in[8];
-  const float* w1 = (const float*)d_in[9];
-  const float* b1 = (const float*)d_in[10];
-  const float* w2 = (const float*)d_in[11];
-  const float* b2 = (const float*)d_in[12];
-  const float* tau = (const float*)d_in[13];
-  float* out = (float*)d_out;
-
   const size_t NX = (size_t)2048 * EE;
   const size_t NW = (size_t)4 * EE * EE;
   const size_t NQK = (size_t)BB * NH * SS * HD;
@@ -636,13 +615,32 @@
   float* T = t_un + (size_t)BB * SS * SS;
   float* rowred = T + 8192;
 
-  k_prep<<<256, 256, 0, stream>>>(Wq, Wk, Wv, Wo, Wth, Wtl);
-  k_qkv_mfma<<<dim3(8, 32, 3), 256, 0, stream>>>(x, Wth, Wtl, bq, bk, bv, w1,
-                                                 b1, w2, b2, T, qh, ql, kh, kl,
-                                                 vth, vtl);
-  k_scores_mfma<<<dim3(8, 8, 32), 256, 0, stream>>>(qh, ql, kh, kl, s);
-  k_rowstat<<<2048, 64, 0, stream>>>(s, T, ma, t_un, rowred);
-  k_av_fused<<<dim3(16, 32), 256, 0, stream>>>(s, ma, t_un, rowred, tau, vth,
-                                               vtl, oh, ol);
-  k_out_mfma<<<dim3(8, 32), 256, 0, stream>>>(oh, ol, Wth, Wtl, bo, out);
-}
+  Params prm;
+  prm.x = (const float*)d_in[0];
+  prm.Wq = (const float*)d_in[1];
+  prm.bq = (const float*)d_in[2];
+  prm.Wk = (const float*)d_in[3];
+  prm.bk = (const float*)d_in[4];
+  prm.Wv = (const float*)d_in[5];
+  prm.bv = (const float*)d_in[6];
+  prm.Wo = (const float*)d_in[7];
+  prm.bo = (const float*)d_in[8];
+  prm.w1 = (const float*)d_in[9];
+  prm.b1 = (const float*)d_in[10];
+  prm.w2 = (const float*)d_in[11];
+  prm.b2 = (const float*)d_in[12];
+  prm.tau = (const float*)d_in[13];
+  prm.out = (float*)d_out;
+  prm.Wth = Wth;  prm.Wtl = Wtl;
+  prm.qh = qh;    prm.ql = ql;
+  prm.kh = kh;    prm.kl = kl;
+  prm.vth = vth;  prm.vtl = vtl;
+  prm.oh = oh;    prm.ol = ol;
+  prm.s = s;      prm.ma = ma;
+  prm.t_un = t_un; prm.T = T;
+  prm.rowred = rowred;
+
+  void* args[] = {&prm};
+  hipLaunchCooperativeKernel((void*)k_fused, dim3(512), dim3(256), args, 0,
+                             stream);
+}
```

Result: slower. 493.5 us (+207.9%).
